# Kernel tuning notes

Hardware: AMD Instinct MI355X
Metric: run time of the kernel (lower is better)

## Reference

```python
import jax, jax.numpy as jnp
import numpy as np

B, H, W = 2, 32, 128
HW = H * W
N, C = 4096, 64
KQ, KN = 32, 16          # nsample_q, nsample
DIST = 10.0              # neighbor distance threshold
NEG = -1e10


def _knn(q, p, k):
    # q: (B,M,3), p: (B,N,3) -> idx (B,M,k), sqdist (B,M,k)
    sqd = jnp.sum((q[:, :, None, :] - p[:, None, :, :]) ** 2, axis=-1)
    neg, idx = jax.lax.top_k(-sqd, k)
    return idx, -neg


def _gather(p, idx):
    # p: (B,N,C), idx: (B,M,K) -> (B,M,K,C)
    return jax.vmap(lambda a, i: a[i])(p, idx)


def _norm_feat(x):
    # per-point channel normalization, torch.std default is unbiased (ddof=1)
    m = jnp.mean(x, axis=-1, keepdims=True)
    s = jnp.clip(jnp.std(x, axis=-1, keepdims=True, ddof=1), 1e-12)
    return (x - m) / s


def _conv(x, w, b, g, e):
    # 1x1 conv + BatchNorm (track_running_stats=False -> batch stats) + LeakyReLU(0.1)
    y = jnp.einsum('bnkc,cd->bnkd', x, w) + b
    mu = y.mean(axis=(0, 1, 2), keepdims=True)
    var = y.var(axis=(0, 1, 2), keepdims=True)
    y = (y - mu) * jax.lax.rsqrt(var + 1e-5) * g + e
    return jnp.where(y > 0, y, 0.1 * y)


def setup_inputs() -> dict:
    key = jax.random.key(0)
    ks = jax.random.split(key, 20)
    inp = {
        'xyz_proj_raw': jax.random.normal(ks[0], (B, H, W, 3), jnp.float32),
        'warped_xyz': jax.random.normal(ks[1], (B, HW, 3), jnp.float32),
        'warped_points': jax.random.normal(ks[2], (B, HW, C), jnp.float32),
        'idx_n2': jax.random.randint(ks[3], (B, HW, 2), 0, W),
        'f2_xyz': jax.random.normal(ks[4], (B, N, 3), jnp.float32),
        'f2_points': jax.random.normal(ks[5], (B, N, C), jnp.float32),
        'lidar_z': jax.random.uniform(ks[6], (B, HW, 1), jnp.float32),
    }
    shapes = {
        'm1w0': (70, 128), 'm1w1': (128, 64), 'piw': (6, 64),
        'm2w0': (128, 64), 'm2w1': (64, 64), 'pcw': (10, 64),
        'm3w0': (192, 64), 'm3w1': (64, 64),
    }
    i = 7
    for name, shp in shapes.items():
        inp[name] = jax.random.normal(ks[i], shp, jnp.float32) * 0.05
        i += 1
        pre = name[:-2] if name[-2] == 'w' else name[:-1]
        suf = name[-1] if name[-2] == 'w' else ''
        cout = shp[1]
        inp[pre + 'b' + suf] = jnp.zeros((cout,), jnp.float32)
        inp[pre + 'g' + suf] = jnp.ones((cout,), jnp.float32)
        inp[pre + 'e' + suf] = jnp.zeros((cout,), jnp.float32)
    return inp


def reference(xyz_proj_raw, warped_xyz, warped_points, idx_n2, f2_xyz, f2_points, lidar_z,
              m1w0, m1b0, m1g0, m1e0, m1w1, m1b1, m1g1, m1e1,
              piw, pib, pig, pie,
              m2w0, m2b0, m2g0, m2e0, m2w1, m2b1, m2g1, m2e1,
              pcw, pcb, pcg, pce,
              m3w0, m3b0, m3g0, m3e0, m3w1, m3b1, m3g1, m3e1):
    # ---- stage 1: cross kNN grouping into image features ----
    idx_q, _ = _knn(warped_xyz, f2_xyz, KQ)
    qi_xyz = _gather(f2_xyz, idx_q)          # (B,HW,KQ,3)
    qi_pts = _gather(f2_points, idx_q)       # (B,HW,KQ,C)

    wxyz = warped_xyz * lidar_z              # (B,HW,3)
    pi_xyz_exp = jnp.broadcast_to(wxyz[:, :, None, :], (B, HW, KQ, 3))
    pi_pts_exp = jnp.broadcast_to(warped_points[:, :, None, :], (B, HW, KQ, C))
    pi_xyz_diff_concat = jnp.concatenate([pi_xyz_exp, qi_xyz], axis=3)  # (B,HW,KQ,6)

    pi_feat_diff = _norm_feat(pi_pts_exp) * _norm_feat(qi_pts)          # correlation
    feat = jnp.concatenate([pi_xyz_diff_concat, pi_feat_diff], axis=3)  # (B,HW,KQ,70)

    feat = _conv(feat, m1w0, m1b0, m1g0, m1e0)
    feat = _conv(feat, m1w1, m1b1, m1g1, m1e1)                          # (B,HW,KQ,64)
    pi_enc = _conv(pi_xyz_diff_concat, piw, pib, pig, pie)              # (B,HW,KQ,64)

    pi_cat = jnp.concatenate([pi_enc, feat], axis=3)
    pi_cat = _conv(pi_cat, m2w0, m2b0, m2g0, m2e0)
    pi_cat = _conv(pi_cat, m2w1, m2b1, m2g1, m2e1)
    WQ = jax.nn.softmax(pi_cat, axis=2)
    pi_feat1 = jnp.sum(WQ * feat, axis=2)                               # (B,HW,64)

    # ---- stage 2: self kNN (use_trans=False -> raw projected xyz), thresholded validity ----
    xyz_pr = xyz_proj_raw.reshape(B, HW, 3)
    idx2, sqd2 = _knn(xyz_pr, xyz_pr, KN)
    valid = (sqd2 < DIST * DIST).astype(pi_feat1.dtype)[..., None]      # (B,HW,KN,1)

    pc_xyz_g = _gather(wxyz, idx2)                                      # (B,HW,KN,3)
    pc_pts_g = _gather(pi_feat1, idx2)                                  # (B,HW,KN,64)
    pc_xyz_new = jnp.broadcast_to(wxyz[:, :, None, :], (B, HW, KN, 3))
    pc_pts_new = jnp.broadcast_to(warped_points[:, :, None, :], (B, HW, KN, C))

    pc_diff = pc_xyz_g - pc_xyz_new
    pc_euc = jnp.sqrt(jnp.sum(pc_diff * pc_diff, axis=3, keepdims=True) + 1e-20)
    pc_xyz_cat = jnp.concatenate([pc_xyz_new, pc_xyz_g, pc_diff, pc_euc], axis=3)  # 10ch

    pc_enc = _conv(pc_xyz_cat, pcw, pcb, pcg, pce)
    pc_cat = jnp.concatenate([pc_enc, pc_pts_new, pc_pts_g], axis=-1)   # (B,HW,KN,192)
    pc_cat = _conv(pc_cat, m3w0, m3b0, m3g0, m3e0)
    pc_cat = _conv(pc_cat, m3w1, m3b1, m3g1, m3e1)

    pc_cat = pc_cat * valid + NEG * (1.0 - valid)
    WP = jax.nn.softmax(pc_cat, axis=2)
    out = jnp.sum(WP * pc_pts_g, axis=2)                                # (B,HW,64)
    return out.reshape(B, H, W, -1)
```

## Files before the change

### kernel.cpp

```cpp
#include <hip/hip_runtime.h>
#include <math.h>

constexpr int Bn  = 2;
constexpr int HWn = 4096;
constexpr int Nn  = 4096;
constexpr int KQn = 32;
constexpr int KNn = 16;
constexpr float INV_R1 = 1.0f/262144.0f;
constexpr float INV_R2 = 1.0f/131072.0f;

typedef _Float16 f16x8 __attribute__((ext_vector_type(8)));
typedef _Float16 f16x2 __attribute__((ext_vector_type(2)));
typedef float    f32x4 __attribute__((ext_vector_type(4)));

__device__ __forceinline__ float wred64(float v){
  #pragma unroll
  for (int m = 32; m > 0; m >>= 1) v += __shfl_xor(v, m, 64);
  return v;
}
__device__ __forceinline__ float leakyf(float v){ return v > 0.f ? v : 0.1f*v; }

__device__ __forceinline__ void bn_param(const float* st, int c, float inv_n,
                                         const float* g, const float* e,
                                         float& sc, float& sh){
  float mu  = st[c]*inv_n;
  float var = st[128+c]*inv_n - mu*mu;
  float s   = g[c]*rsqrtf(var + 1e-5f);
  sc = s; sh = e[c] - mu*s;
}

constexpr int XT_LD = 104;
__device__ __forceinline__ void build_xtile(
    int m0, const float* __restrict__ wxyz, const float* __restrict__ f2_xyz,
    const float* __restrict__ normW, const float* __restrict__ normF2,
    const int* __restrict__ idxq, _Float16* __restrict__ xt, int tid)
{
  int r = tid >> 2, q = tid & 3;
  int row = m0 + r;
  int p = row >> 5, b = p >> 12;
  int idx = idxq[row];
  unsigned int* d32 = (unsigned int*)(xt + r*XT_LD);
  union { unsigned int u; _Float16 h[2]; } pk;
  if (q == 0){
    const float* wx = wxyz + (size_t)p*3;
    const float* fx = f2_xyz + ((size_t)b*Nn + idx)*3;
    pk.h[0]=(_Float16)wx[0]; pk.h[1]=(_Float16)wx[1]; d32[0]=pk.u;
    pk.h[0]=(_Float16)wx[2]; pk.h[1]=(_Float16)fx[0]; d32[1]=pk.u;
    pk.h[0]=(_Float16)fx[1]; pk.h[1]=(_Float16)fx[2]; d32[2]=pk.u;
  }
  const float4* nw = (const float4*)(normW  + (size_t)p*64) + q*4;
  const float4* nf = (const float4*)(normF2 + ((size_t)b*Nn + idx)*64) + q*4;
  #pragma unroll
  for (int i=0;i<4;i++){
    float4 a = nw[i], f = nf[i];
    int base = 3 + q*8 + i*2;
    pk.h[0]=(_Float16)(a.x*f.x); pk.h[1]=(_Float16)(a.y*f.y); d32[base]=pk.u;
    pk.h[0]=(_Float16)(a.z*f.z); pk.h[1]=(_Float16)(a.w*f.w); d32[base+1]=pk.u;
  }
  if (q == 3){
    #pragma unroll
    for (int c=35;c<48;c++) d32[c] = 0u;
  }
}

__device__ __forceinline__ void build_x10(int row,
    const float* __restrict__ wxyz, const int* __restrict__ idx2, float* x){
  int p = row >> 4, b = p >> 12;
  int idx = idx2[row];
  const float* nw = wxyz + (size_t)p*3;
  const float* gw = wxyz + ((size_t)b*HWn + idx)*3;
  float n0=nw[0],n1=nw[1],n2=nw[2];
  float g0=gw[0],g1=gw[1],g2=gw[2];
  float d0=g0-n0, d1=g1-n1, d2=g2-n2;
  x[0]=n0;x[1]=n1;x[2]=n2; x[3]=g0;x[4]=g1;x[5]=g2;
  x[6]=d0;x[7]=d1;x[8]=d2; x[9]=sqrtf(d0*d0+d1*d1+d2*d2+1e-20f);
}

__global__ __launch_bounds__(256) void k_knn_prep(
    const float* __restrict__ qA, const float* __restrict__ pA, int* __restrict__ oA,
    const float* __restrict__ qB, const float* __restrict__ pB, int* __restrict__ oB,
    float* __restrict__ ovalid,
    const float* __restrict__ lidar_z,
    const float* __restrict__ warped_points, const float* __restrict__ f2_points,
    const float* __restrict__ m1w0, const float* __restrict__ m1w1,
    const float* __restrict__ piw, const float* __restrict__ pcw,
    const float* __restrict__ m2w0, const float* __restrict__ m2w1,
    const float* __restrict__ m3w0, const float* __restrict__ m3w1,
    float* __restrict__ wxyz, float* __restrict__ normW, float* __restrict__ normF2,
    float* __restrict__ piwT, float* __restrict__ pcwT,
    _Float16* __restrict__ w1h, _Float16* __restrict__ w2h,
    _Float16* __restrict__ w3h, _Float16* __restrict__ w4h,
    _Float16* __restrict__ w5h, _Float16* __restrict__ w6h)
{
  int bid = blockIdx.x;
  int tid = threadIdx.x;
  if (bid >= 16384){
    int blk = bid - 16384;
    if (blk < 4096){
      int lane = tid & 63;
      int p = blk*4 + (tid >> 6);
      const float* src; float* dst;
      if (p < Bn*HWn){ src = warped_points + (size_t)p*64; dst = normW + (size_t)p*64; }
      else { int q = p - Bn*HWn; src = f2_points + (size_t)q*64; dst = normF2 + (size_t)q*64; }
      float x = src[lane];
      float m = wred64(x) * (1.f/64.f);
      float d = x - m;
      float ss = wred64(d*d);
      float s = fmaxf(sqrtf(ss*(1.f/63.f)), 1e-12f);
      dst[lane] = d / s;
    } else if (blk < 4192){
      int e = (blk-4096)*256 + tid;
      wxyz[e] = qA[e] * lidar_z[e/3];
    } else if (blk < 4196){
      int e = (blk-4192)*256 + tid;
      if (e < 384){ piwT[(e & 63)*6  + (e >> 6)] = piw[e]; }
      else if (e < 1024){ int f = e-384; pcwT[(f & 63)*10 + (f >> 6)] = pcw[f]; }
    } else {
      int e = (blk-4196)*256 + tid;
      if (e < 12288){
        int j = e/96, k = e - j*96;
        w1h[e] = (k < 70) ? (_Float16)m1w0[k*128 + j] : (_Float16)0.f;
      } else if (e < 20480){
        int f = e - 12288; int d = f >> 7, c = f & 127;
        w2h[f] = (_Float16)m1w1[c*64 + d];
      } else if (e < 28672){
        int f = e - 20480; int d = f >> 7, c = f & 127;
        w3h[f] = (_Float16)m2w0[c*64 + d];
      } else if (e < 32768){
        int f = e - 28672; int d = f >> 6, c = f & 63;
        w4h[f] = (_Float16)m2w1[c*64 + d];
      } else if (e < 45056){
        int f = e - 32768; int d = f/192, c = f - 192*d;
        w5h[f] = (_Float16)m3w0[c*64 + d];
      } else {
        int f = e - 45056; int d = f >> 6, c = f & 63;
        w6h[f] = (_Float16)m3w1[c*64 + d];
      }
    }
    return;
  }
  __shared__ int hist[4096];
  __shared__ int wsum[4];
  __shared__ unsigned int redm[4], redM[4];
  __shared__ int sh_sel, sh_rem, sh_cls, cnt_lt, cnt_eq;
  bool second = bid >= 8192;
  int blk = second ? (bid - 8192) : bid;
  int K = second ? KNn : KQn;
  const float* qpts = second ? qB : qA;
  const float* pts  = second ? pB : pA;
  int* oidx = second ? oB : oA;
  int b = blk >> 12;
  int qi = blk & 4095;
  int lane = tid & 63, wv = tid >> 6;
  const float* qp = qpts + ((size_t)(b*HWn+qi))*3;
  float qx=qp[0], qy=qp[1], qz=qp[2];
  const float* pb = pts + (size_t)b*Nn*3;
  unsigned int key[16];
  {
    const float4* pb4 = (const float4*)(pb + (size_t)tid*48);
    float4 v[12];
    #pragma unroll
    for (int i=0;i<12;i++) v[i] = pb4[i];
    const float* f = (const float*)v;
    #pragma unroll
    for (int i=0;i<16;i++){
      float dx = __fsub_rn(qx, f[i*3+0]);
      float dy = __fsub_rn(qy, f[i*3+1]);
      float dz = __fsub_rn(qz, f[i*3+2]);
      float d2 = __fadd_rn(__fadd_rn(__fmul_rn(dx,dx), __fmul_rn(dy,dy)), __fmul_rn(dz,dz));
      key[i] = __float_as_uint(d2);
    }
  }
  {
    int4 z = {0,0,0,0};
    #pragma unroll
    for (int j=0;j<2;j++) ((int4*)hist)[tid + j*256] = z;
  }
  unsigned int mn = key[0], mx = key[0];
  #pragma unroll
  for (int i=1;i<16;i++){ mn = min(mn, key[i]); mx = max(mx, key[i]); }
  #pragma unroll
  for (int m=32;m>0;m>>=1){
    mn = min(mn, (unsigned int)__shfl_xor((int)mn, m, 64));
    mx = max(mx, (unsigned int)__shfl_xor((int)mx, m, 64));
  }
  if (lane == 0){ redm[wv] = mn; redM[wv] = mx; }
  if (tid == 0){ cnt_lt = 0; cnt_eq = 0; }
  __syncthreads();
  mn = min(min(redm[0],redm[1]), min(redm[2],redm[3]));
  mx = max(max(redM[0],redM[1]), max(redM[2],redM[3]));
  unsigned int R = mx - mn;
  int L = (R == 0u) ? 0 : (31 - __clz(R));
  int shift = (L > 10) ? (L - 10) : 0;
  #pragma unroll
  for (int i=0;i<16;i++){
    unsigned int d = ((key[i]-mn) >> shift) & 2047u;
    int slot = (int)(((d & 7u) << 8) | (d >> 3));
    atomicAdd(&hist[slot], 1);
  }
  __syncthreads();
  {
    int hv[8]; int tot = 0;
    #pragma unroll
    for (int i=0;i<8;i++){ hv[i] = hist[tid + i*256]; tot += hv[i]; }
    int pref = tot;
    #pragma unroll
    for (int m=1;m<64;m<<=1){ int t = __shfl_up(pref, m, 64); if (lane >= m) pref += t; }
    if (lane == 63) wsum[wv] = pref;
    __syncthreads();
    int off = 0;
    #pragma unroll
    for (int i=0;i<3;i++) if (i < wv) off += wsum[i];
    pref += off;
    if (pref >= K && (pref - tot) < K){
      int running = pref - tot;
      bool done = false;
      #pragma unroll
      for (int i=0;i<8;i++){
        if (!done && running + hv[i] >= K){
          sh_sel = tid*8 + i;
          sh_rem = K - running;
          sh_cls = hv[i];
          done = true;
        }
        if (!done) running += hv[i];
      }
    }
  }
  __syncthreads();
  unsigned int sel = (unsigned int)sh_sel;
  int rem = sh_rem, cls = sh_cls;
  int nless = K - rem;
  size_t obase = ((size_t)(b*HWn+qi))*K;
  const unsigned int U100 = __float_as_uint(100.0f);
  #pragma unroll
  for (int i=0;i<16;i++){
    unsigned int d = ((key[i]-mn) >> shift) & 2047u;
    if (d < sel){
      int s = atomicAdd(&cnt_lt, 1);
      oidx[obase+s] = tid*16 + i;
      if (second) ovalid[obase+s] = (key[i] < U100) ? 1.f : 0.f;
    } else if (d == sel){
      int s = atomicAdd(&cnt_eq, 1);
      if (s < 2048){ hist[s] = (int)key[i]; hist[2048+s] = tid*16 + i; }
    }
  }
  __syncthreads();
  if (wv == 0){
    int cc = cls < 2048 ? cls : 2048;
    for (int c = lane; c < cc; c += 64){
      unsigned int kc = (unsigned int)hist[c];
      int ic = hist[2048+c];
      int rank = 0;
      for (int j = 0; j < cc; j++){
        unsigned int kj = (unsigned int)hist[j];
        if (kj < kc || (kj == kc && hist[2048+j] < ic)) rank++;
      }
      if (rank < rem){
        oidx[obase + nless + rank] = ic;
        if (second) ovalid[obase + nless + rank] = (kc < U100) ? 1.f : 0.f;
      }
    }
  }
}

__global__ __launch_bounds__(256) void k_build_stats(
    const float* __restrict__ wxyz, const float* __restrict__ f2_xyz,
    const float* __restrict__ normW, const float* __restrict__ normF2,
    const int* __restrict__ idxq, const int* __restrict__ idx2,
    const _Float16* __restrict__ w1h,
    float* stats, float* __restrict__ gram)
{
  __shared__ float sacc[66];
  int blk = blockIdx.x, tid = threadIdx.x, lane = tid & 63;
  if (blk < 1024){
    __shared__ _Float16 xt[64*XT_LD];
    __shared__ float ssum[128], sssq[128];
    if (tid < 128){ ssum[tid]=0.f; sssq[tid]=0.f; }
    int wave = tid >> 6;
    int quad = lane >> 4, n16 = lane & 15;
    float r1[8], r2[8];
    #pragma unroll
    for (int i=0;i<8;i++){ r1[i]=0.f; r2[i]=0.f; }
    for (int t=0;t<4;t++){
      build_xtile(blk*256 + t*64, wxyz, f2_xyz, normW, normF2, idxq, xt, tid);
      __syncthreads();
      const _Float16* xr = xt + (size_t)(wave*16 + n16)*XT_LD + quad*8;
      f16x8 a0 = *(const f16x8*)(xr);
      f16x8 a1 = *(const f16x8*)(xr + 32);
      f16x8 a2 = *(const f16x8*)(xr + 64);
      #pragma unroll
      for (int nt = 0; nt < 8; nt++){
        const _Float16* wr = w1h + (size_t)(nt*16 + n16)*96 + quad*8;
        f16x8 b0 = *(const f16x8*)(wr);
        f16x8 b1 = *(const f16x8*)(wr + 32);
        f16x8 b2 = *(const f16x8*)(wr + 64);
        f32x4 acc = {0.f,0.f,0.f,0.f};
        acc = __builtin_amdgcn_mfma_f32_16x16x32_f16(a0, b0, acc, 0,0,0);
        acc = __builtin_amdgcn_mfma_f32_16x16x32_f16(a1, b1, acc, 0,0,0);
        acc = __builtin_amdgcn_mfma_f32_16x16x32_f16(a2, b2, acc, 0,0,0);
        float s1 = acc[0]+acc[1]+acc[2]+acc[3];
        float s2 = acc[0]*acc[0]+acc[1]*acc[1]+acc[2]*acc[2]+acc[3]*acc[3];
        s1 += __shfl_xor(s1, 16, 64); s1 += __shfl_xor(s1, 32, 64);
        s2 += __shfl_xor(s2, 16, 64); s2 += __shfl_xor(s2, 32, 64);
        r1[nt] += s1; r2[nt] += s2;
      }
      __syncthreads();
    }
    if (quad == 0){
      #pragma unroll
      for (int nt=0;nt<8;nt++){
        atomicAdd(&ssum[nt*16+n16], r1[nt]); atomicAdd(&sssq[nt*16+n16], r2[nt]);
      }
    }
    __syncthreads();
    if (tid < 128){ atomicAdd(&stats[tid], ssum[tid]); atomicAdd(&stats[128+tid], sssq[tid]); }
  } else if (blk < 1088){
    float a[28];
    #pragma unroll
    for (int q=0;q<28;q++) a[q]=0.f;
    int g = (blk-1024)*256 + tid;
    for (int s=0;s<16;s++){
      int row = g + s*16384;
      int p = row >> 5, b = p >> 12;
      int idx = idxq[row];
      const float* wx = wxyz + (size_t)p*3;
      const float* fx = f2_xyz + ((size_t)b*Nn + idx)*3;
      float xt7[7] = {wx[0],wx[1],wx[2],fx[0],fx[1],fx[2],1.f};
      int q=0;
      #pragma unroll
      for (int i=0;i<7;i++)
        #pragma unroll
        for (int j=i;j<7;j++) a[q++] += xt7[i]*xt7[j];
    }
    if (tid < 28) sacc[tid]=0.f;
    __syncthreads();
    #pragma unroll
    for (int q=0;q<28;q++){
      float v = wred64(a[q]);
      if (lane==0) atomicAdd(&sacc[q], v);
    }
    __syncthreads();
    if (tid < 28) atomicAdd(&gram[tid], sacc[tid]);
  } else {
    float a[66];
    #pragma unroll
    for (int q=0;q<66;q++) a[q]=0.f;
    int g = (blk-1088)*256 + tid;
    for (int s=0;s<16;s++){
      int row = g + s*8192;
      float x[10];
      build_x10(row, wxyz, idx2, x);
      float xt11[11] = {x[0],x[1],x[2],x[3],x[4],x[5],x[6],x[7],x[8],x[9],1.f};
      int q=0;
      #pragma unroll
      for (int i=0;i<11;i++)
        #pragma unroll
        for (int j=i;j<11;j++) a[q++] += xt11[i]*xt11[j];
    }
    if (tid < 66) sacc[tid]=0.f;
    __syncthreads();
    #pragma unroll
    for (int q=0;q<66;q++){
      float v = wred64(a[q]);
      if (lane==0) atomicAdd(&sacc[q], v);
    }
    __syncthreads();
    if (tid < 66) atomicAdd(&gram[32+tid], sacc[tid]);
  }
}

__global__ __launch_bounds__(256) void k_mfma_m1(
    const float* __restrict__ wxyz, const float* __restrict__ f2_xyz,
    const float* __restrict__ normW, const float* __restrict__ normF2,
    const int* __restrict__ idxq,
    const _Float16* __restrict__ w1h, const _Float16* __restrict__ w2h,
    const float* __restrict__ m1g0, const float* __restrict__ m1e0,
    float* stats, _Float16* __restrict__ y2h,
    const float* __restrict__ gram,
    const float* __restrict__ piw, const float* __restrict__ pib,
    const float* __restrict__ pcw, const float* __restrict__ pcb)
{
  if (blockIdx.x >= 1024){
    int tid = threadIdx.x;
    if (tid < 64){
      int c = tid;
      float wt[7];
      #pragma unroll
      for (int i=0;i<6;i++) wt[i] = piw[i*64+c];
      wt[6] = pib[c];
      const float* G = gram;
      float sum=0.f, ssq=0.f;
      #pragma unroll
      for (int i=0;i<7;i++){
        int offi = i*7 - (i*(i-1))/2;
        sum += wt[i]*G[offi + (6-i)];
        #pragma unroll
        for (int j=0;j<7;j++){
          int ii = i<j? i : j, jj = i<j? j : i;
          int o = ii*7 - (ii*(ii-1))/2 + (jj-ii);
          ssq += wt[i]*wt[j]*G[o];
        }
      }
      stats[2*256+c] = sum; stats[2*256+128+c] = ssq;
    } else if (tid < 128){
      int c = tid-64;
      float wt[11];
      #pragma unroll
      for (int i=0;i<10;i++) wt[i] = pcw[i*64+c];
      wt[10] = pcb[c];
      const float* G = gram + 32;
      float sum=0.f, ssq=0.f;
      #pragma unroll
      for (int i=0;i<11;i++){
        int offi = i*11 - (i*(i-1))/2;
        sum += wt[i]*G[offi + (10-i)];
        #pragma unroll
        for (int j=0;j<11;j++){
          int ii = i<j? i : j, jj = i<j? j : i;
          int o = ii*11 - (ii*(ii-1))/2 + (jj-ii);
          ssq += wt[i]*wt[j]*G[o];
        }
      }
      stats[5*256+c] = sum; stats[5*256+128+c] = ssq;
    }
    return;
  }
  __shared__ _Float16 xt[64*XT_LD];
  __shared__ _Float16 st[64*136];
  __shared__ float sc1[128], sh1[128], ssum[64], sssq[64];
  int tid = threadIdx.x;
  if (tid < 128){
    float s,h; bn_param(stats, tid, INV_R1, m1g0, m1e0, s, h);
    sc1[tid]=s; sh1[tid]=h;
  }
  if (tid < 64){ ssum[tid]=0.f; sssq[tid]=0.f; }
  int wave = tid >> 6, lane = tid & 63;
  int quad = lane >> 4, n16 = lane & 15;
  float r1[4], r2[4];
  #pragma unroll
  for (int i=0;i<4;i++){ r1[i]=0.f; r2[i]=0.f; }
  for (int t=0;t<4;t++){
    build_xtile(blockIdx.x*256 + t*64, wxyz, f2_xyz, normW, normF2, idxq, xt, tid);
    __syncthreads();
    const _Float16* xr = xt + (size_t)(wave*16 + n16)*XT_LD + quad*8;
    f16x8 a0 = *(const f16x8*)(xr);
    f16x8 a1 = *(const f16x8*)(xr + 32);
    f16x8 a2 = *(const f16x8*)(xr + 64);
    #pragma unroll
    for (int nt = 0; nt < 8; nt++){
      const _Float16* wr = w1h + (size_t)(nt*16 + n16)*96 + quad*8;
      f16x8 b0 = *(const f16x8*)(wr);
      f16x8 b1 = *(const f16x8*)(wr + 32);
      f16x8 b2 = *(const f16x8*)(wr + 64);
      f32x4 acc = {0.f,0.f,0.f,0.f};
      acc = __builtin_amdgcn_mfma_f32_16x16x32_f16(a0, b0, acc, 0,0,0);
      acc = __builtin_amdgcn_mfma_f32_16x16x32_f16(a1, b1, acc, 0,0,0);
      acc = __builtin_amdgcn_mfma_f32_16x16x32_f16(a2, b2, acc, 0,0,0);
      int ch = nt*16 + n16;
      float sc = sc1[ch], sh = sh1[ch];
      #pragma unroll
      for (int r=0;r<4;r++){
        float v = leakyf(acc[r]*sc + sh);
        st[(size_t)(wave*16 + quad*4 + r)*136 + ch] = (_Float16)v;
      }
    }
    __syncthreads();
    const _Float16* tr = st + (size_t)(wave*16 + n16)*136 + quad*8;
    f16x8 t0 = *(const f16x8*)(tr);
    f16x8 t1 = *(const f16x8*)(tr + 32);
    f16x8 t2 = *(const f16x8*)(tr + 64);
    f16x8 t3 = *(const f16x8*)(tr + 96);
    #pragma unroll
    for (int nt = 0; nt < 4; nt++){
      const _Float16* wr = w2h + (size_t)(nt*16 + n16)*128 + quad*8;
      f16x8 b0 = *(const f16x8*)(wr);
      f16x8 b1 = *(const f16x8*)(wr + 32);
      f16x8 b2 = *(const f16x8*)(wr + 64);
      f16x8 b3 = *(const f16x8*)(wr + 96);
      f32x4 acc = {0.f,0.f,0.f,0.f};
      acc = __builtin_amdgcn_mfma_f32_16x16x32_f16(t0, b0, acc, 0,0,0);
      acc = __builtin_amdgcn_mfma_f32_16x16x32_f16(t1, b1, acc, 0,0,0);
      acc = __builtin_amdgcn_mfma_f32_16x16x32_f16(t2, b2, acc, 0,0,0);
      acc = __builtin_amdgcn_mfma_f32_16x16x32_f16(t3, b3, acc, 0,0,0);
      int ch = nt*16 + n16;
      #pragma unroll
      for (int r=0;r<4;r++){
        int rowg = blockIdx.x*256 + t*64 + wave*16 + quad*4 + r;
        y2h[(size_t)rowg*64 + ch] = (_Float16)acc[r];
      }
      float s1 = acc[0]+acc[1]+acc[2]+acc[3];
      float s2 = acc[0]*acc[0]+acc[1]*acc[1]+acc[2]*acc[2]+acc[3]*acc[3];
      s1 += __shfl_xor(s1, 16, 64); s1 += __shfl_xor(s1, 32, 64);
      s2 += __shfl_xor(s2, 16, 64); s2 += __shfl_xor(s2, 32, 64);
      r1[nt] += s1; r2[nt] += s2;
    }
  }
  __syncthreads();
  if (quad == 0){
    #pragma unroll
    for (int nt=0;nt<4;nt++){
      atomicAdd(&ssum[nt*16+n16], r1[nt]); atomicAdd(&sssq[nt*16+n16], r2[nt]);
    }
  }
  __syncthreads();
  if (tid < 64){ atomicAdd(&stats[1*256+tid], ssum[tid]); atomicAdd(&stats[1*256+128+tid], sssq[tid]); }
}

__global__ __launch_bounds__(256) void k_mfma_m2a(
    const float* __restrict__ wxyz, const float* __restrict__ f2_xyz,
    const int* __restrict__ idxq,
    const float* __restrict__ piwT, const float* __restrict__ pib,
    const float* __restrict__ pig, const float* __restrict__ pie,
    const float* __restrict__ m1g1, const float* __restrict__ m1e1,
    const _Float16* __restrict__ y2h, const _Float16* __restrict__ w3h,
    float* stats, _Float16* __restrict__ y3h)
{
  __shared__ _Float16 su[64*136];
  __shared__ float spw[384];
  __shared__ float scp[64], shp[64], sc2[64], sh2[64], ssum[64], sssq[64];
  int tid = threadIdx.x;
  for (int d = tid; d < 384; d += 256) spw[d] = piwT[d];
  if (tid < 64){
    float s,h;
    bn_param(stats+2*256, tid, INV_R1, pig,  pie,  s, h); scp[tid]=s; shp[tid]=h;
    bn_param(stats+1*256, tid, INV_R1, m1g1, m1e1, s, h); sc2[tid]=s; sh2[tid]=h;
    ssum[tid]=0.f; sssq[tid]=0.f;
  }
  __syncthreads();
  int r = tid & 63, cg = tid >> 6;
  int wave = tid >> 6, lane = tid & 63, quad = lane >> 4, n16 = lane & 15;
  float r1[4], r2[4];
  #pragma unroll
  for (int i=0;i<4;i++){ r1[i]=0.f; r2[i]=0.f; }
  for (int t=0;t<4;t++){
    int rowg = blockIdx.x*256 + t*64 + r;
    {
      int p = rowg >> 5, b = p >> 12;
      int idx = idxq[rowg];
      const float* wx = wxyz + (size_t)p*3;
      const float* fx = f2_xyz + ((size_t)b*Nn + idx)*3;
      float x0=wx[0],x1=wx[1],x2=wx[2],x3=fx[0],x4=fx[1],x5=fx[2];
      #pragma unroll
      for (int jj=0;jj<16;jj++){
        int j = cg*16 + jj;
        const float* pw = spw + j*6;
        float e = pib[j] + x0*pw[0]+x1*pw[1]+x2*pw[2]+x3*pw[3]+x4*pw[4]+x5*pw[5];
        su[r*136 + j] = (_Float16)leakyf(e*scp[j] + shp[j]);
      }
      const f16x8* yr = (const f16x8*)(y2h + (size_t)rowg*64 + cg*16);
      f16x8 q0 = yr[0], q1 = yr[1];
      #pragma unroll
      for (int jj=0;jj<8;jj++){
        int c = cg*16 + jj;
        su[r*136 + 64 + c] = (_Float16)leakyf((float)q0[jj]*sc2[c] + sh2[c]);
      }
      #pragma unroll
      for (int jj=0;jj<8;jj++){
        int c = cg*16 + 8 + jj;
        su[r*136 + 64 + c] = (_Float16)leakyf((float)q1[jj]*sc2[c] + sh2[c]);
      }
    }
    __syncthreads();
    const _Float16* ur = su + (size_t)(wave*16 + n16)*136 + quad*8;
    f16x8 a0 = *(const f16x8*)(ur);
    f16x8 a1 = *(const f16x8*)(ur + 32);
    f16x8 a2 = *(const f16x8*)(ur + 64);
    f16x8 a3 = *(const f16x8*)(ur + 96);
    #pragma unroll
    for (int nt = 0; nt < 4; nt++){
      const _Float16* wr = w3h + (size_t)(nt*16 + n16)*128 + quad*8;
      f16x8 b0 = *(const f16x8*)(wr);
      f16x8 b1 = *(const f16x8*)(wr + 32);
      f16x8 b2 = *(const f16x8*)(wr + 64);
      f16x8 b3 = *(const f16x8*)(wr + 96);
      f32x4 acc = {0.f,0.f,0.f,0.f};
      acc = __builtin_amdgcn_mfma_f32_16x16x32_f16(a0, b0, acc, 0,0,0);
      acc = __builtin_amdgcn_mfma_f32_16x16x32_f16(a1, b1, acc, 0,0,0);
      acc = __builtin_amdgcn_mfma_f32_16x16x32_f16(a2, b2, acc, 0,0,0);
      acc = __builtin_amdgcn_mfma_f32_16x16x32_f16(a3, b3, acc, 0,0,0);
      int ch = nt*16 + n16;
      #pragma unroll
      for (int rr=0;rr<4;rr++){
        int rg = blockIdx.x*256 + t*64 + wave*16 + quad*4 + rr;
        y3h[(size_t)rg*64 + ch] = (_Float16)acc[rr];
      }
      float s1 = acc[0]+acc[1]+acc[2]+acc[3];
      float s2 = acc[0]*acc[0]+acc[1]*acc[1]+acc[2]*acc[2]+acc[3]*acc[3];
      s1 += __shfl_xor(s1, 16, 64); s1 += __shfl_xor(s1, 32, 64);
      s2 += __shfl_xor(s2, 16, 64); s2 += __shfl_xor(s2, 32, 64);
      r1[nt] += s1; r2[nt] += s2;
    }
    __syncthreads();
  }
  if (quad == 0){
    #pragma unroll
    for (int nt=0;nt<4;nt++){
      atomicAdd(&ssum[nt*16+n16], r1[nt]); atomicAdd(&sssq[nt*16+n16], r2[nt]);
    }
  }
  __syncthreads();
  if (tid < 64){ atomicAdd(&stats[3*256+tid], ssum[tid]); atomicAdd(&stats[3*256+128+tid], sssq[tid]); }
}

__global__ __launch_bounds__(256) void k_mfma_pw64(
    const _Float16* __restrict__ yin, const _Float16* __restrict__ wh,
    const float* __restrict__ g, const float* __restrict__ e,
    const float* statsIn, float* statsOut, float inv_n,
    _Float16* __restrict__ yout)
{
  __shared__ _Float16 stt[64*72];
  __shared__ float sc[64], sh[64], ssum[64], sssq[64];
  int tid = threadIdx.x;
  if (tid < 64){
    float s,h; bn_param(statsIn, tid, inv_n, g, e, s, h);
    sc[tid]=s; sh[tid]=h; ssum[tid]=0.f; sssq[tid]=0.f;
  }
  __syncthreads();
  int r = tid & 63, cg = tid >> 6;
  int wave = tid >> 6, lane = tid & 63, quad = lane >> 4, n16 = lane & 15;
  float r1[4], r2[4];
  #pragma unroll
  for (int i=0;i<4;i++){ r1[i]=0.f; r2[i]=0.f; }
  for (int t=0;t<4;t++){
    int rowg = blockIdx.x*256 + t*64 + r;
    const f16x8* yr = (const f16x8*)(yin + (size_t)rowg*64 + cg*16);
    f16x8 q0 = yr[0], q1 = yr[1];
    #pragma unroll
    for (int jj=0;jj<8;jj++){
      int c = cg*16 + jj;
      stt[r*72 + c] = (_Float16)leakyf((float)q0[jj]*sc[c] + sh[c]);
    }
    #pragma unroll
    for (int jj=0;jj<8;jj++){
      int c = cg*16 + 8 + jj;
      stt[r*72 + c] = (_Float16)leakyf((float)q1[jj]*sc[c] + sh[c]);
    }
    __syncthreads();
    const _Float16* tr = stt + (size_t)(wave*16 + n16)*72 + quad*8;
    f16x8 a0 = *(const f16x8*)(tr);
    f16x8 a1 = *(const f16x8*)(tr + 32);
    #pragma unroll
    for (int nt = 0; nt < 4; nt++){
      const _Float16* wr = wh + (size_t)(nt*16 + n16)*64 + quad*8;
      f16x8 b0 = *(const f16x8*)(wr);
      f16x8 b1 = *(const f16x8*)(wr + 32);
      f32x4 acc = {0.f,0.f,0.f,0.f};
      acc = __builtin_amdgcn_mfma_f32_16x16x32_f16(a0, b0, acc, 0,0,0);
      acc = __builtin_amdgcn_mfma_f32_16x16x32_f16(a1, b1, acc, 0,0,0);
      int ch = nt*16 + n16;
      #pragma unroll
      for (int rr=0;rr<4;rr++){
        int rg = blockIdx.x*256 + t*64 + wave*16 + quad*4 + rr;
        yout[(size_t)rg*64 + ch] = (_Float16)acc[rr];
      }
      float s1 = acc[0]+acc[1]+acc[2]+acc[3];
      float s2 = acc[0]*acc[0]+acc[1]*acc[1]+acc[2]*acc[2]+acc[3]*acc[3];
      s1 += __shfl_xor(s1, 16, 64); s1 += __shfl_xor(s1, 32, 64);
      s2 += __shfl_xor(s2, 16, 64); s2 += __shfl_xor(s2, 32, 64);
      r1[nt] += s1; r2[nt] += s2;
    }
    __syncthreads();
  }
  if (quad == 0){
    #pragma unroll
    for (int nt=0;nt<4;nt++){
      atomicAdd(&ssum[nt*16+n16], r1[nt]); atomicAdd(&sssq[nt*16+n16], r2[nt]);
    }
  }
  __syncthreads();
  if (tid < 64){ atomicAdd(&statsOut[tid], ssum[tid]); atomicAdd(&statsOut[128+tid], sssq[tid]); }
}

__global__ __launch_bounds__(256) void k_mfma_m3a(
    const float* __restrict__ wxyz, const float* __restrict__ warped_points,
    const _Float16* __restrict__ pif1h, const int* __restrict__ idx2,
    const float* __restrict__ pcwT, const float* __restrict__ pcb,
    const float* __restrict__ pcg, const float* __restrict__ pce,
    const _Float16* __restrict__ w5h,
    float* stats, _Float16* __restrict__ y5h)
{
  __shared__ _Float16 sv[64*200];
  __shared__ float spw[640];
  __shared__ float scp[64], shp[64], ssum[64], sssq[64];
  int tid = threadIdx.x;
  for (int d = tid; d < 640; d += 256) spw[d] = pcwT[d];
  if (tid < 64){
    float s,h; bn_param(stats+5*256, tid, INV_R2, pcg, pce, s, h);
    scp[tid]=s; shp[tid]=h; ssum[tid]=0.f; sssq[tid]=0.f;
  }
  __syncthreads();
  int r = tid & 63, cg = tid >> 6;
  int wave = tid >> 6, lane = tid & 63, quad = lane >> 4, n16 = lane & 15;
  float r1[4], r2[4];
  #pragma unroll
  for (int i=0;i<4;i++){ r1[i]=0.f; r2[i]=0.f; }
  for (int t=0;t<4;t++){
    int rowg = blockIdx.x*256 + t*64 + r;
    {
      int p = rowg >> 4, b = p >> 12;
      int idx = idx2[rowg];
      float x[10];
      build_x10(rowg, wxyz, idx2, x);
      #pragma unroll
      for (int jj=0;jj<16;jj++){
        int j = cg*16 + jj;
        const float* pw = spw + j*10;
        float e = pcb[j];
        #pragma unroll
        for (int i=0;i<10;i++) e += x[i]*pw[i];
        sv[r*200 + j] = (_Float16)leakyf(e*scp[j] + shp[j]);
      }
      const float4* wp = (const float4*)(warped_points + (size_t)p*64 + cg*16);
      #pragma unroll
      for (int v4=0; v4<4; v4++){
        float4 q = wp[v4];
        int c = 64 + cg*16 + v4*4;
        sv[r*200 + c + 0] = (_Float16)q.x;
        sv[r*200 + c + 1] = (_Float16)q.y;
        sv[r*200 + c + 2] = (_Float16)q.z;
        sv[r*200 + c + 3] = (_Float16)q.w;
      }
      const f16x8* pg = (const f16x8*)(pif1h + ((size_t)(b*HWn) + idx)*64 + cg*16);
      f16x8 g0 = pg[0], g1 = pg[1];
      #pragma unroll
      for (int jj=0;jj<8;jj++) sv[r*200 + 128 + cg*16 + jj] = g0[jj];
      #pragma unroll
      for (int jj=0;jj<8;jj++) sv[r*200 + 136 + cg*16 + jj] = g1[jj];
    }
    __syncthreads();
    const _Float16* vr = sv + (size_t)(wave*16 + n16)*200 + quad*8;
    f16x8 a0 = *(const f16x8*)(vr);
    f16x8 a1 = *(const f16x8*)(vr + 32);
    f16x8 a2 = *(const f16x8*)(vr + 64);
    f16x8 a3 = *(const f16x8*)(vr + 96);
    f16x8 a4 = *(const f16x8*)(vr + 128);
    f16x8 a5 = *(const f16x8*)(vr + 160);
    #pragma unroll
    for (int nt = 0; nt < 4; nt++){
      const _Float16* wr = w5h + (size_t)(nt*16 + n16)*192 + quad*8;
      f32x4 acc = {0.f,0.f,0.f,0.f};
      acc = __builtin_amdgcn_mfma_f32_16x16x32_f16(a0, *(const f16x8*)(wr),       acc, 0,0,0);
      acc = __builtin_amdgcn_mfma_f32_16x16x32_f16(a1, *(const f16x8*)(wr + 32),  acc, 0,0,0);
      acc = __builtin_amdgcn_mfma_f32_16x16x32_f16(a2, *(const f16x8*)(wr + 64),  acc, 0,0,0);
      acc = __builtin_amdgcn_mfma_f32_16x16x32_f16(a3, *(const f16x8*)(wr + 96),  acc, 0,0,0);
      acc = __builtin_amdgcn_mfma_f32_16x16x32_f16(a4, *(const f16x8*)(wr + 128), acc, 0,0,0);
      acc = __builtin_amdgcn_mfma_f32_16x16x32_f16(a5, *(const f16x8*)(wr + 160), acc, 0,0,0);
      int ch = nt*16 + n16;
      #pragma unroll
      for (int rr=0;rr<4;rr++){
        int rg = blockIdx.x*256 + t*64 + wave*16 + quad*4 + rr;
        y5h[(size_t)rg*64 + ch] = (_Float16)acc[rr];
      }
      float s1 = acc[0]+acc[1]+acc[2]+acc[3];
      float s2 = acc[0]*acc[0]+acc[1]*acc[1]+acc[2]*acc[2]+acc[3]*acc[3];
      s1 += __shfl_xor(s1, 16, 64); s1 += __shfl_xor(s1, 32, 64);
      s2 += __shfl_xor(s2, 16, 64); s2 += __shfl_xor(s2, 32, 64);
      r1[nt] += s1; r2[nt] += s2;
    }
    __syncthreads();
  }
  if (quad == 0){
    #pragma unroll
    for (int nt=0;nt<4;nt++){
      atomicAdd(&ssum[nt*16+n16], r1[nt]); atomicAdd(&sssq[nt*16+n16], r2[nt]);
    }
  }
  __syncthreads();
  if (tid < 64){ atomicAdd(&stats[6*256+tid], ssum[tid]); atomicAdd(&stats[6*256+128+tid], sssq[tid]); }
}

__global__ __launch_bounds__(256) void k_softmax1(
    const _Float16* __restrict__ y2h, const _Float16* __restrict__ y4h,
    const float* stats,
    const float* __restrict__ m1g1, const float* __restrict__ m1e1,
    const float* __restrict__ m2g1, const float* __restrict__ m2e1,
    _Float16* __restrict__ pif1h)
{
  int tid = threadIdx.x;
  int p  = blockIdx.x*8 + (tid >> 5);
  int dp = tid & 31;
  int d0 = 2*dp, d1 = 2*dp + 1;
  float sc2a,sh2a,sc4a,sh4a, sc2b,sh2b,sc4b,sh4b;
  bn_param(stats+1*256, d0, INV_R1, m1g1, m1e1, sc2a, sh2a);
  bn_param(stats+4*256, d0, INV_R1, m2g1, m2e1, sc4a, sh4a);
  bn_param(stats+1*256, d1, INV_R1, m1g1, m1e1, sc2b, sh2b);
  bn_param(stats+4*256, d1, INV_R1, m2g1, m2e1, sc4b, sh4b);
  size_t rb = (size_t)p*KQn;
  const _Float16* y4base = y4h + rb*64 + d0;
  const _Float16* y2base = y2h + rb*64 + d0;
  float va[32], vb[32];
  float mxa = -1e30f, mxb = -1e30f;
  #pragma unroll
  for (int k=0;k<32;k++){
    f16x2 h = *(const f16x2*)(y4base + (size_t)k*64);
    float ta = leakyf((float)h[0]*sc4a + sh4a);
    float tb = leakyf((float)h[1]*sc4b + sh4b);
    va[k] = ta; mxa = fmaxf(mxa, ta);
    vb[k] = tb; mxb = fmaxf(mxb, tb);
  }
  float sea = 0.f, seb = 0.f;
  #pragma unroll
  for (int k=0;k<32;k++){
    float ea = __expf(va[k]-mxa); va[k]=ea; sea += ea;
    float eb = __expf(vb[k]-mxb); vb[k]=eb; seb += eb;
  }
  float inva = 1.f/sea, invb = 1.f/seb;
  float acca = 0.f, accb = 0.f;
  #pragma unroll
  for (int k=0;k<32;k++){
    f16x2 h = *(const f16x2*)(y2base + (size_t)k*64);
    acca += va[k]*leakyf((float)h[0]*sc2a + sh2a);
    accb += vb[k]*leakyf((float)h[1]*sc2b + sh2b);
  }
  f16x2 o; o[0] = (_Float16)(acca*inva); o[1] = (_Float16)(accb*invb);
  *(f16x2*)(pif1h + (size_t)p*64 + d0) = o;
}

__global__ __launch_bounds__(256) void k_softmax2(
    const _Float16* __restrict__ y6h, const _Float16* __restrict__ pif1h,
    const int* __restrict__ idx2, const float* __restrict__ validf,
    const float* stats,
    const float* __restrict__ m3g1, const float* __restrict__ m3e1,
    float* __restrict__ out)
{
  int tid = threadIdx.x;
  int p  = blockIdx.x*8 + (tid >> 5);
  int b  = p >> 12;
  int dp = tid & 31;
  int d0 = 2*dp, d1 = 2*dp + 1;
  float sca,sha,scb,shb;
  bn_param(stats+7*256, d0, INV_R2, m3g1, m3e1, sca, sha);
  bn_param(stats+7*256, d1, INV_R2, m3g1, m3e1, scb, shb);
  size_t rb = (size_t)p*KNn;
  const _Float16* y6base = y6h + rb*64 + d0;
  float va[16], vb[16];
  float mxa = -1e30f, mxb = -1e30f;
  #pragma unroll
  for (int k=0;k<16;k++){
    f16x2 h = *(const f16x2*)(y6base + (size_t)k*64);
    bool ok = validf[rb+k] > 0.5f;
    float ta = ok ? leakyf((float)h[0]*sca + sha) : -1e10f;
    float tb = ok ? leakyf((float)h[1]*scb + shb) : -1e10f;
    va[k] = ta; mxa = fmaxf(mxa, ta);
    vb[k] = tb; mxb = fmaxf(mxb, tb);
  }
  float sea = 0.f, seb = 0.f;
  #pragma unroll
  for (int k=0;k<16;k++){
    float ea = __expf(va[k]-mxa); va[k]=ea; sea += ea;
    float eb = __expf(vb[k]-mxb); vb[k]=eb; seb += eb;
  }
  float inva = 1.f/sea, invb = 1.f/seb;
  float acca = 0.f, accb = 0.f;
  #pragma unroll
  for (int k=0;k<16;k++){
    int idx = idx2[rb+k];
    f16x2 h = *(const f16x2*)(pif1h + ((size_t)(b*HWn) + idx)*64 + d0);
    acca += va[k]*(float)h[0];
    accb += vb[k]*(float)h[1];
  }
  float2 o; o.x = acca*inva; o.y = accb*invb;
  *(float2*)(out + (size_t)p*64 + d0) = o;
}

extern "C" void kernel_launch(void* const* d_in, const int* in_sizes, int n_in,
                              void* d_out, int out_size, void* d_ws, size_t ws_size,
                              hipStream_t stream)
{
  (void)in_sizes; (void)n_in; (void)out_size; (void)ws_size;
  const float* xyz_proj      = (const float*)d_in[0];
  const float* warped_xyz    = (const float*)d_in[1];
  const float* warped_points = (const float*)d_in[2];
  const float* f2_xyz        = (const float*)d_in[4];
  const float* f2_points     = (const float*)d_in[5];
  const float* lidar_z       = (const float*)d_in[6];
  const float* m1w0=(const float*)d_in[7],  *m1g0=(const float*)d_in[9],  *m1e0=(const float*)d_in[10];
  const float* m1w1=(const float*)d_in[11], *m1g1=(const float*)d_in[13], *m1e1=(const float*)d_in[14];
  const float* piw =(const float*)d_in[15], *pib =(const float*)d_in[16], *pig =(const float*)d_in[17], *pie =(const float*)d_in[18];
  const float* m2w0=(const float*)d_in[19], *m2g0=(const float*)d_in[21], *m2e0=(const float*)d_in[22];
  const float* m2w1=(const float*)d_in[23], *m2g1=(const float*)d_in[25], *m2e1=(const float*)d_in[26];
  const float* pcw =(const float*)d_in[27], *pcb =(const float*)d_in[28], *pcg =(const float*)d_in[29], *pce =(const float*)d_in[30];
  const float* m3w0=(const float*)d_in[31], *m3g0=(const float*)d_in[33], *m3e0=(const float*)d_in[34];
  const float* m3w1=(const float*)d_in[35], *m3g1=(const float*)d_in[37], *m3e1=(const float*)d_in[38];
  float* out = (float*)d_out;

  float* ws     = (float*)d_ws;
  float* wxyz   = ws;
  float* normW  = wxyz   + 24576;
  float* normF2 = normW  + 524288;
  float* piwT   = normF2 + 524288;
  float* pcwT   = piwT   + 384;
  float* stats  = pcwT   + 640;
  float* gram   = stats  + 2048;
  int*   idxq   = (int*)(gram + 128);
  int*   idx2   = idxq   + 262144;
  float* validf = (float*)(idx2 + 131072);
  _Float16* pif1h = (_Float16*)(validf + 131072);
  float* X1f    = validf + 131072 + 524288;
  float* y2f    = X1f + 12582912;
  _Float16* y2h = (_Float16*)y2f;
  float* y3f    = y2f + 8388608;
  _Float16* y3h = (_Float16*)y3f;
  float* whb    = y3f + 8388608;
  _Float16* w1h = (_Float16*)whb;
  _Float16* w2h = w1h + 12288;
  _Float16* w3h = w2h + 8192;
  _Float16* w4h = w3h + 8192;
  _Float16* w5h = w4h + 4096;
  _Float16* w6h = w5h + 12288;
  _Float16* y4h = (_Float16*)X1f;
  _Float16* y5h = (_Float16*)(X1f + 8388608);
  _Float16* y6h = y3h;

  hipMemsetAsync(stats, 0, (2048+128)*sizeof(float), stream);
  k_knn_prep<<<20772,256,0,stream>>>(warped_xyz, f2_xyz, idxq,
                                     xyz_proj, xyz_proj, idx2, validf,
                                     lidar_z, warped_points, f2_points,
                                     m1w0, m1w1, piw, pcw, m2w0, m2w1, m3w0, m3w1,
                                     wxyz, normW, normF2, piwT, pcwT,
                                     w1h, w2h, w3h, w4h, w5h, w6h);
  k_build_stats<<<1120,256,0,stream>>>(wxyz, f2_xyz, normW, normF2, idxq, idx2,
                                       w1h, stats, gram);
  k_mfma_m1<<<1025,256,0,stream>>>(wxyz, f2_xyz, normW, normF2, idxq,
                                   w1h, w2h, m1g0, m1e0, stats, y2h,
                                   gram, piw, pib, pcw, pcb);
  k_mfma_m2a<<<1024,256,0,stream>>>(wxyz, f2_xyz, idxq, piwT, pib, pig, pie,
                                    m1g1, m1e1, y2h, w3h, stats, y3h);
  k_mfma_pw64<<<1024,256,0,stream>>>(y3h, w4h, m2g0, m2e0,
                                     stats+3*256, stats+4*256, INV_R1, y4h);
  k_softmax1<<<1024,256,0,stream>>>(y2h, y4h, stats, m1g1, m1e1, m2g1, m2e1, pif1h);
  k_mfma_m3a<<<512,256,0,stream>>>(wxyz, warped_points, pif1h, idx2,
                                   pcwT, pcb, pcg, pce, w5h, stats, y5h);
  k_mfma_pw64<<<512,256,0,stream>>>(y5h, w6h, m3g0, m3e0,
                                    stats+6*256, stats+7*256, INV_R2, y6h);
  k_softmax2<<<1024,256,0,stream>>>(y6h, pif1h, idx2, validf, stats, m3g1, m3e1, out);
}
```

Baseline: 492.5 us.

## Fuse post-KNN kernel chain into one cooperative persistent kernel with grid syncs

Replaces the eight separate launches that follow the KNN prep (stats, m1, m2a, pw64, softmax1, m3a, pw64, softmax2) with a single cooperative kernel of 512 blocks. Each phase loops over work items and the phases are separated by grid.sync and thread fences, with a shared-memory arena reused across phases. The aim is to remove per-launch overhead and inter-kernel gaps. In exchange, occupancy is capped at 512 persistent blocks, a grid-wide barrier is paid at every phase, and some cross-phase stores use atomics. A fallback path with separate kernels runs when a cooperative launch is not possible.

Measured after the change: 572.3 us. 16.2% more time.

```diff
diff --git a/kernel.cpp b/kernel.cpp
--- a/kernel.cpp
+++ b/kernel.cpp
@@ -1,5 +1,8 @@
 #include <hip/hip_runtime.h>
+#include <hip/hip_cooperative_groups.h>
 #include <math.h>
+
+namespace cg = cooperative_groups;
 
 constexpr int Bn  = 2;
 constexpr int HWn = 4096;
@@ -264,18 +267,30 @@
   }
 }
 
-__global__ __launch_bounds__(256) void k_build_stats(
-    const float* __restrict__ wxyz, const float* __restrict__ f2_xyz,
-    const float* __restrict__ normW, const float* __restrict__ normF2,
-    const int* __restrict__ idxq, const int* __restrict__ idx2,
-    const _Float16* __restrict__ w1h,
-    float* stats, float* __restrict__ gram)
-{
-  __shared__ float sacc[66];
-  int blk = blockIdx.x, tid = threadIdx.x, lane = tid & 63;
+struct ChainArgs {
+  const float *wxyz, *f2_xyz, *normW, *normF2;
+  const int *idxq, *idx2;
+  const _Float16 *w1h, *w2h, *w3h, *w4h, *w5h, *w6h;
+  float *stats, *gram;
+  const float *piwT, *pcwT;
+  const float *piw, *pib, *pig, *pie;
+  const float *pcw, *pcb, *pcg, *pce;
+  const float *m1g0, *m1e0, *m1g1, *m1e1;
+  const float *m2g0, *m2e0, *m2g1, *m2e1;
+  const float *m3g0, *m3e0, *m3g1, *m3e1;
+  const float *warped_points, *validf;
+  _Float16 *y2h, *y3h, *y4h, *y5h, *y6h, *pif1h;
+  float *out;
+};
+
+constexpr int ARENA = 29440;
+
+__device__ void phase0(const ChainArgs& A, char* sm, int blk, int tid){
+  int lane = tid & 63;
   if (blk < 1024){
-    __shared__ _Float16 xt[64*XT_LD];
-    __shared__ float ssum[128], sssq[128];
+    _Float16* xt  = (_Float16*)sm;
+    float* ssum = (float*)(sm + 13312);
+    float* sssq = (float*)(sm + 13824);
     if (tid < 128){ ssum[tid]=0.f; sssq[tid]=0.f; }
     int wave = tid >> 6;
     int quad = lane >> 4, n16 = lane & 15;
@@ -283,7 +298,7 @@
     #pragma unroll
     for (int i=0;i<8;i++){ r1[i]=0.f; r2[i]=0.f; }
     for (int t=0;t<4;t++){
-      build_xtile(blk*256 + t*64, wxyz, f2_xyz, normW, normF2, idxq, xt, tid);
+      build_xtile(blk*256 + t*64, A.wxyz, A.f2_xyz, A.normW, A.normF2, A.idxq, xt, tid);
       __syncthreads();
       const _Float16* xr = xt + (size_t)(wave*16 + n16)*XT_LD + quad*8;
       f16x8 a0 = *(const f16x8*)(xr);
@@ -291,7 +306,7 @@
       f16x8 a2 = *(const f16x8*)(xr + 64);
       #pragma unroll
       for (int nt = 0; nt < 8; nt++){
-        const _Float16* wr = w1h + (size_t)(nt*16 + n16)*96 + quad*8;
+        const _Float16* wr = A.w1h + (size_t)(nt*16 + n16)*96 + quad*8;
         f16x8 b0 = *(const f16x8*)(wr);
         f16x8 b1 = *(const f16x8*)(wr + 32);
         f16x8 b2 = *(const f16x8*)(wr + 64);
@@ -314,8 +329,9 @@
       }
     }
     __syncthreads();
-    if (tid < 128){ atomicAdd(&stats[tid], ssum[tid]); atomicAdd(&stats[128+tid], sssq[tid]); }
+    if (tid < 128){ atomicAdd(&A.stats[tid], ssum[tid]); atomicAdd(&A.stats[128+tid], sssq[tid]); }
   } else if (blk < 1088){
+    float* sacc = (float*)(sm + 14336);
     float a[28];
     #pragma unroll
     for (int q=0;q<28;q++) a[q]=0.f;
@@ -323,9 +339,9 @@
     for (int s=0;s<16;s++){
       int row = g + s*16384;
       int p = row >> 5, b = p >> 12;
-      int idx = idxq[row];
-      const float* wx = wxyz + (size_t)p*3;
-      const float* fx = f2_xyz + ((size_t)b*Nn + idx)*3;
+      int idx = A.idxq[row];
+      const float* wx = A.wxyz + (size_t)p*3;
+      const float* fx = A.f2_xyz + ((size_t)b*Nn + idx)*3;
       float xt7[7] = {wx[0],wx[1],wx[2],fx[0],fx[1],fx[2],1.f};
       int q=0;
       #pragma unroll
@@ -341,8 +357,10 @@
       if (lane==0) atomicAdd(&sacc[q], v);
     }
     __syncthreads();
-    if (tid < 28) atomicAdd(&gram[tid], sacc[tid]);
+    if (tid < 28) atomicAdd(&A.gram[tid], sacc[tid]);
+    __syncthreads();
   } else {
+    float* sacc = (float*)(sm + 14336);
     float a[66];
     #pragma unroll
     for (int q=0;q<66;q++) a[q]=0.f;
@@ -350,7 +368,7 @@
     for (int s=0;s<16;s++){
       int row = g + s*8192;
       float x[10];
-      build_x10(row, wxyz, idx2, x);
+      build_x10(row, A.wxyz, A.idx2, x);
       float xt11[11] = {x[0],x[1],x[2],x[3],x[4],x[5],x[6],x[7],x[8],x[9],1.f};
       int q=0;
       #pragma unroll
@@ -366,72 +384,66 @@
       if (lane==0) atomicAdd(&sacc[q], v);
     }
     __syncthreads();
-    if (tid < 66) atomicAdd(&gram[32+tid], sacc[tid]);
-  }
-}
-
-__global__ __launch_bounds__(256) void k_mfma_m1(
-    const float* __restrict__ wxyz, const float* __restrict__ f2_xyz,
-    const float* __restrict__ normW, const float* __restrict__ normF2,
-    const int* __restrict__ idxq,
-    const _Float16* __restrict__ w1h, const _Float16* __restrict__ w2h,
-    const float* __restrict__ m1g0, const float* __restrict__ m1e0,
-    float* stats, _Float16* __restrict__ y2h,
-    const float* __restrict__ gram,
-    const float* __restrict__ piw, const float* __restrict__ pib,
-    const float* __restrict__ pcw, const float* __restrict__ pcb)
-{
-  if (blockIdx.x >= 1024){
-    int tid = threadIdx.x;
-    if (tid < 64){
-      int c = tid;
-      float wt[7];
-      #pragma unroll
-      for (int i=0;i<6;i++) wt[i] = piw[i*64+c];
-      wt[6] = pib[c];
-      const float* G = gram;
-      float sum=0.f, ssq=0.f;
-      #pragma unroll
-      for (int i=0;i<7;i++){
-        int offi = i*7 - (i*(i-1))/2;
-        sum += wt[i]*G[offi + (6-i)];
-        #pragma unroll
-        for (int j=0;j<7;j++){
-          int ii = i<j? i : j, jj = i<j? j : i;
-          int o = ii*7 - (ii*(ii-1))/2 + (jj-ii);
-          ssq += wt[i]*wt[j]*G[o];
-        }
-      }
-      stats[2*256+c] = sum; stats[2*256+128+c] = ssq;
-    } else if (tid < 128){
-      int c = tid-64;
-      float wt[11];
-      #pragma unroll
-      for (int i=0;i<10;i++) wt[i] = pcw[i*64+c];
-      wt[10] = pcb[c];
-      const float* G = gram + 32;
-      float sum=0.f, ssq=0.f;
-      #pragma unroll
-      for (int i=0;i<11;i++){
-        int offi = i*11 - (i*(i-1))/2;
-        sum += wt[i]*G[offi + (10-i)];
-        #pragma unroll
-        for (int j=0;j<11;j++){
-          int ii = i<j? i : j, jj = i<j? j : i;
-          int o = ii*11 - (ii*(ii-1))/2 + (jj-ii);
-          ssq += wt[i]*wt[j]*G[o];
-        }
-      }
-      stats[5*256+c] = sum; stats[5*256+128+c] = ssq;
-    }
-    return;
-  }
-  __shared__ _Float16 xt[64*XT_LD];
-  __shared__ _Float16 st[64*136];
-  __shared__ float sc1[128], sh1[128], ssum[64], sssq[64];
-  int tid = threadIdx.x;
+    if (tid < 66) atomicAdd(&A.gram[32+tid], sacc[tid]);
+    __syncthreads();
+  }
+}
+
+__device__ void gram_fin(const ChainArgs& A, int tid){
+  if (tid < 64){
+    int c = tid;
+    float wt[7];
+    #pragma unroll
+    for (int i=0;i<6;i++) wt[i] = A.piw[i*64+c];
+    wt[6] = A.pib[c];
+    const float* G = A.gram;
+    float sum=0.f, ssq=0.f;
+    #pragma unroll
+    for (int i=0;i<7;i++){
+      int offi = i*7 - (i*(i-1))/2;
+      sum += wt[i]*G[offi + (6-i)];
+      #pragma unroll
+      for (int j=0;j<7;j++){
+        int ii = i<j? i : j, jj = i<j? j : i;
+        int o = ii*7 - (ii*(ii-1))/2 + (jj-ii);
+        ssq += wt[i]*wt[j]*G[o];
+      }
+    }
+    __hip_atomic_store(&A.stats[2*256+c], sum, __ATOMIC_RELAXED, __HIP_MEMORY_SCOPE_AGENT);
+    __hip_atomic_store(&A.stats[2*256+128+c], ssq, __ATOMIC_RELAXED, __HIP_MEMORY_SCOPE_AGENT);
+  } else if (tid < 128){
+    int c = tid-64;
+    float wt[11];
+    #pragma unroll
+    for (int i=0;i<10;i++) wt[i] = A.pcw[i*64+c];
+    wt[10] = A.pcb[c];
+    const float* G = A.gram + 32;
+    float sum=0.f, ssq=0.f;
+    #pragma unroll
+    for (int i=0;i<11;i++){
+      int offi = i*11 - (i*(i-1))/2;
+      sum += wt[i]*G[offi + (10-i)];
+      #pragma unroll
+      for (int j=0;j<11;j++){
+        int ii = i<j? i : j, jj = i<j? j : i;
+        int o = ii*11 - (ii*(ii-1))/2 + (jj-ii);
+        ssq += wt[i]*wt[j]*G[o];
+      }
+    }
+    __hip_atomic_store(&A.stats[5*256+c], sum, __ATOMIC_RELAXED, __HIP_MEMORY_SCOPE_AGENT);
+    __hip_atomic_store(&A.stats[5*256+128+c], ssq, __ATOMIC_RELAXED, __HIP_MEMORY_SCOPE_AGENT);
+  }
+}
+
+__device__ void phase1_m1(const ChainArgs& A, char* sm, int w, int tid){
+  _Float16* xt  = (_Float16*)sm;
+  _Float16* st  = (_Float16*)sm;
+  float* sc1  = (float*)(sm + 17408);
+  float* sh1  = (float*)(sm + 17920);
+  float* ssum = (float*)(sm + 18432);
+  float* sssq = (float*)(sm + 18688);
   if (tid < 128){
-    float s,h; bn_param(stats, tid, INV_R1, m1g0, m1e0, s, h);
+    float s,h; bn_param(A.stats, tid, INV_R1, A.m1g0, A.m1e0, s, h);
     sc1[tid]=s; sh1[tid]=h;
   }
   if (tid < 64){ ssum[tid]=0.f; sssq[tid]=0.f; }
@@ -441,15 +453,16 @@
   #pragma unroll
   for (int i=0;i<4;i++){ r1[i]=0.f; r2[i]=0.f; }
   for (int t=0;t<4;t++){
-    build_xtile(blockIdx.x*256 + t*64, wxyz, f2_xyz, normW, normF2, idxq, xt, tid);
+    build_xtile(w*256 + t*64, A.wxyz, A.f2_xyz, A.normW, A.normF2, A.idxq, xt, tid);
     __syncthreads();
     const _Float16* xr = xt + (size_t)(wave*16 + n16)*XT_LD + quad*8;
     f16x8 a0 = *(const f16x8*)(xr);
     f16x8 a1 = *(const f16x8*)(xr + 32);
     f16x8 a2 = *(const f16x8*)(xr + 64);
+    __syncthreads();
     #pragma unroll
     for (int nt = 0; nt < 8; nt++){
-      const _Float16* wr = w1h + (size_t)(nt*16 + n16)*96 + quad*8;
+      const _Float16* wr = A.w1h + (size_t)(nt*16 + n16)*96 + quad*8;
       f16x8 b0 = *(const f16x8*)(wr);
       f16x8 b1 = *(const f16x8*)(wr + 32);
       f16x8 b2 = *(const f16x8*)(wr + 64);
@@ -473,7 +486,7 @@
     f16x8 t3 = *(const f16x8*)(tr + 96);
     #pragma unroll
     for (int nt = 0; nt < 4; nt++){
-      const _Float16* wr = w2h + (size_t)(nt*16 + n16)*128 + quad*8;
+      const _Float16* wr = A.w2h + (size_t)(nt*16 + n16)*128 + quad*8;
       f16x8 b0 = *(const f16x8*)(wr);
       f16x8 b1 = *(const f16x8*)(wr + 32);
       f16x8 b2 = *(const f16x8*)(wr + 64);
@@ -486,8 +499,8 @@
       int ch = nt*16 + n16;
       #pragma unroll
       for (int r=0;r<4;r++){
-        int rowg = blockIdx.x*256 + t*64 + wave*16 + quad*4 + r;
-        y2h[(size_t)rowg*64 + ch] = (_Float16)acc[r];
+        int rowg = w*256 + t*64 + wave*16 + quad*4 + r;
+        A.y2h[(size_t)rowg*64 + ch] = (_Float16)acc[r];
       }
       float s1 = acc[0]+acc[1]+acc[2]+acc[3];
       float s2 = acc[0]*acc[0]+acc[1]*acc[1]+acc[2]*acc[2]+acc[3]*acc[3];
@@ -495,8 +508,8 @@
       s2 += __shfl_xor(s2, 16, 64); s2 += __shfl_xor(s2, 32, 64);
       r1[nt] += s1; r2[nt] += s2;
     }
-  }
-  __syncthreads();
+    __syncthreads();
+  }
   if (quad == 0){
     #pragma unroll
     for (int nt=0;nt<4;nt++){
@@ -504,60 +517,56 @@
     }
   }
   __syncthreads();
-  if (tid < 64){ atomicAdd(&stats[1*256+tid], ssum[tid]); atomicAdd(&stats[1*256+128+tid], sssq[tid]); }
-}
-
-__global__ __launch_bounds__(256) void k_mfma_m2a(
-    const float* __restrict__ wxyz, const float* __restrict__ f2_xyz,
-    const int* __restrict__ idxq,
-    const float* __restrict__ piwT, const float* __restrict__ pib,
-    const float* __restrict__ pig, const float* __restrict__ pie,
-    const float* __restrict__ m1g1, const float* __restrict__ m1e1,
-    const _Float16* __restrict__ y2h, const _Float16* __restrict__ w3h,
-    float* stats, _Float16* __restrict__ y3h)
-{
-  __shared__ _Float16 su[64*136];
-  __shared__ float spw[384];
-  __shared__ float scp[64], shp[64], sc2[64], sh2[64], ssum[64], sssq[64];
-  int tid = threadIdx.x;
-  for (int d = tid; d < 384; d += 256) spw[d] = piwT[d];
+  if (tid < 64){ atomicAdd(&A.stats[1*256+tid], ssum[tid]); atomicAdd(&A.stats[1*256+128+tid], sssq[tid]); }
+}
+
+__device__ void phase2_m2a(const ChainArgs& A, char* sm, int w, int tid){
+  _Float16* su = (_Float16*)sm;
+  float* spw = (float*)(sm + 17408);
+  float* scp = (float*)(sm + 18944);
+  float* shp = (float*)(sm + 19200);
+  float* sc2 = (float*)(sm + 19456);
+  float* sh2 = (float*)(sm + 19712);
+  float* ssum = (float*)(sm + 19968);
+  float* sssq = (float*)(sm + 20224);
+  for (int d = tid; d < 384; d += 256) spw[d] = A.piwT[d];
   if (tid < 64){
     float s,h;
-    bn_param(stats+2*256, tid, INV_R1, pig,  pie,  s, h); scp[tid]=s; shp[tid]=h;
-    bn_param(stats+1*256, tid, INV_R1, m1g1, m1e1, s, h); sc2[tid]=s; sh2[tid]=h;
+    bn_param(A.stats+2*256, tid, INV_R1, A.pig,  A.pie,  s, h); scp[tid]=s; shp[tid]=h;
+    bn_param(A.stats+1*256, tid, INV_R1, A.m1g1, A.m1e1, s, h); sc2[tid]=s; sh2[tid]=h;
     ssum[tid]=0.f; sssq[tid]=0.f;
   }
   __syncthreads();
-  int r = tid & 63, cg = tid >> 6;
+  int r = tid & 63, cgp = tid >> 6;
   int wave = tid >> 6, lane = tid & 63, quad = lane >> 4, n16 = lane & 15;
   float r1[4], r2[4];
   #pragma unroll
   for (int i=0;i<4;i++){ r1[i]=0.f; r2[i]=0.f; }
   for (int t=0;t<4;t++){
-    int rowg = blockIdx.x*256 + t*64 + r;
+    int rowg = w*256 + t*64 + r;
     {
       int p = rowg >> 5, b = p >> 12;
-      int idx = idxq[rowg];
-      const float* wx = wxyz + (size_t)p*3;
-      const float* fx = f2_xyz + ((size_t)b*Nn + idx)*3;
+      int idx = A.idxq[rowg];
+      const float* wx = A.wxyz + (size_t)p*3;
+      const float* fx = A.f2_xyz + ((size_t)b*Nn + idx)*3;
       float x0=wx[0],x1=wx[1],x2=wx[2],x3=fx[0],x4=fx[1],x5=fx[2];
       #pragma unroll
       for (int jj=0;jj<16;jj++){
-        int j = cg*16 + jj;
+        int j = cgp*16 + jj;
         const float* pw = spw + j*6;
-        float e = pib[j] + x0*pw[0]+x1*pw[1]+x2*pw[2]+x3*pw[3]+x4*pw[4]+x5*pw[5];
+        float e = A.pib[j] + x0*pw[0]+x1*pw[1]+x2*pw[2]+x3*pw[3]+x4*pw[4]+x5*pw[5];
         su[r*136 + j] = (_Float16)leakyf(e*scp[j] + shp[j]);
       }
-      const f16x8* yr = (const f16x8*)(y2h + (size_t)rowg*64 + cg*16);
+      const f16x8* yr = (const f16x8*)(A.y2h + (size_t)rowg*64 + cgp*16);
       f16x8 q0 = yr[0], q1 = yr[1];
       #pragma unroll
       for (int jj=0;jj<8;jj++){
-        int c = cg*16 + jj;
+        int c = cgp*16 + jj;
         su[r*136 + 64 + c] = (_Float16)leakyf((float)q0[jj]*sc2[c] + sh2[c]);
       }
       #pragma unroll
       for (int jj=0;jj<8;jj++){
-        int c = cg*16 + 8 + jj;
+        int c = cgp*16 + 8 + jj;
         su[r*136 + 64 + c] = (_Float16)leakyf((float)q1[jj]*sc2[c] + sh2[c]);
       }
     }
@@ -569,7 +578,7 @@
     f16x8 a3 = *(const f16x8*)(ur + 96);
     #pragma unroll
     for (int nt = 0; nt < 4; nt++){
-      const _Float16* wr = w3h + (size_t)(nt*16 + n16)*128 + quad*8;
+      const _Float16* wr = A.w3h + (size_t)(nt*16 + n16)*128 + quad*8;
       f16x8 b0 = *(const f16x8*)(wr);
       f16x8 b1 = *(const f16x8*)(wr + 32);
       f16x8 b2 = *(const f16x8*)(wr + 64);
@@ -582,8 +591,8 @@
       int ch = nt*16 + n16;
       #pragma unroll
       for (int rr=0;rr<4;rr++){
-        int rg = blockIdx.x*256 + t*64 + wave*16 + quad*4 + rr;
-        y3h[(size_t)rg*64 + ch] = (_Float16)acc[rr];
+        int rg = w*256 + t*64 + wave*16 + quad*4 + rr;
+        A.y3h[(size_t)rg*64 + ch] = (_Float16)acc[rr];
       }
       float s1 = acc[0]+acc[1]+acc[2]+acc[3];
       float s2 = acc[0]*acc[0]+acc[1]*acc[1]+acc[2]*acc[2]+acc[3]*acc[3];
@@ -600,40 +609,42 @@
     }
   }
   __syncthreads();
-  if (tid < 64){ atomicAdd(&stats[3*256+tid], ssum[tid]); atomicAdd(&stats[3*256+128+tid], sssq[tid]); }
-}
-
-__global__ __launch_bounds__(256) void k_mfma_pw64(
+  if (tid < 64){ atomicAdd(&A.stats[3*256+tid], ssum[tid]); atomicAdd(&A.stats[3*256+128+tid], sssq[tid]); }
+}
+
+__device__ void phase_pw64(char* sm, int w, int tid,
     const _Float16* __restrict__ yin, const _Float16* __restrict__ wh,
     const float* __restrict__ g, const float* __restrict__ e,
     const float* statsIn, float* statsOut, float inv_n,
     _Float16* __restrict__ yout)
 {
-  __shared__ _Float16 stt[64*72];
-  __shared__ float sc[64], sh[64], ssum[64], sssq[64];
-  int tid = threadIdx.x;
+  _Float16* stt = (_Float16*)sm;
+  float* sc  = (float*)(sm + 9216);
+  float* sh  = (float*)(sm + 9472);
+  float* ssum = (float*)(sm + 9728);
+  float* sssq = (float*)(sm + 9984);
   if (tid < 64){
     float s,h; bn_param(statsIn, tid, inv_n, g, e, s, h);
     sc[tid]=s; sh[tid]=h; ssum[tid]=0.f; sssq[tid]=0.f;
   }
   __syncthreads();
-  int r = tid & 63, cg = tid >> 6;
+  int r = tid & 63, cgp = tid >> 6;
   int wave = tid >> 6, lane = tid & 63, quad = lane >> 4, n16 = lane & 15;
   float r1[4], r2[4];
   #pragma unroll
   for (int i=0;i<4;i++){ r1[i]=0.f; r2[i]=0.f; }
   for (int t=0;t<4;t++){
-    int rowg = blockIdx.x*256 + t*64 + r;
-    const f16x8* yr = (const f16x8*)(yin + (size_t)rowg*64 + cg*16);
+    int rowg = w*256 + t*64 + r;
+    const f16x8* yr = (const f16x8*)(yin + (size_t)rowg*64 + cgp*16);
     f16x8 q0 = yr[0], q1 = yr[1];
     #pragma unroll
     for (int jj=0;jj<8;jj++){
-      int c = cg*16 + jj;
+      int c = cgp*16 + jj;
       stt[r*72 + c] = (_Float16)leakyf((float)q0[jj]*sc[c] + sh[c]);
     }
     #pragma unroll
     for (int jj=0;jj<8;jj++){
-      int c = cg*16 + 8 + jj;
+      int c = cgp*16 + 8 + jj;
       stt[r*72 + c] = (_Float16)leakyf((float)q1[jj]*sc[c] + sh[c]);
     }
     __syncthreads();
@@ -651,7 +662,7 @@
       int ch = nt*16 + n16;
       #pragma unroll
       for (int rr=0;rr<4;rr++){
-        int rg = blockIdx.x*256 + t*64 + wave*16 + quad*4 + rr;
+        int rg = w*256 + t*64 + wave*16 + quad*4 + rr;
         yout[(size_t)rg*64 + ch] = (_Float16)acc[rr];
       }
       float s1 = acc[0]+acc[1]+acc[2]+acc[3];
@@ -672,61 +683,56 @@
   if (tid < 64){ atomicAdd(&statsOut[tid], ssum[tid]); atomicAdd(&statsOut[128+tid], sssq[tid]); }
 }
 
-__global__ __launch_bounds__(256) void k_mfma_m3a(
-    const float* __restrict__ wxyz, const float* __restrict__ warped_points,
-    const _Float16* __restrict__ pif1h, const int* __restrict__ idx2,
-    const float* __restrict__ pcwT, const float* __restrict__ pcb,
-    const float* __restrict__ pcg, const float* __restrict__ pce,
-    const _Float16* __restrict__ w5h,
-    float* stats, _Float16* __restrict__ y5h)
-{
-  __shared__ _Float16 sv[64*200];
-  __shared__ float spw[640];
-  __shared__ float scp[64], shp[64], ssum[64], sssq[64];
-  int tid = threadIdx.x;
-  for (int d = tid; d < 640; d += 256) spw[d] = pcwT[d];
+__device__ void phase5_m3a(const ChainArgs& A, char* sm, int w, int tid){
+  _Float16* sv = (_Float16*)sm;
+  float* spw = (float*)(sm + 25600);
+  float* scp = (float*)(sm + 28160);
+  float* shp = (float*)(sm + 28416);
+  float* ssum = (float*)(sm + 28672);
+  float* sssq = (float*)(sm + 28928);
+  for (int d = tid; d < 640; d += 256) spw[d] = A.pcwT[d];
   if (tid < 64){
-    float s,h; bn_param(stats+5*256, tid, INV_R2, pcg, pce, s, h);
+    float s,h; bn_param(A.stats+5*256, tid, INV_R2, A.pcg, A.pce, s, h);
     scp[tid]=s; shp[tid]=h; ssum[tid]=0.f; sssq[tid]=0.f;
   }
   __syncthreads();
-  int r = tid & 63, cg = tid >> 6;
+  int r = tid & 63, cgp = tid >> 6;
   int wave = tid >> 6, lane = tid & 63, quad = lane >> 4, n16 = lane & 15;
   float r1[4], r2[4];
   #pragma unroll
   for (int i=0;i<4;i++){ r1[i]=0.f; r2[i]=0.f; }
   for (int t=0;t<4;t++){
-    int rowg = blockIdx.x*256 + t*64 + r;
+    int rowg = w*256 + t*64 + r;
     {
       int p = rowg >> 4, b = p >> 12;
-      int idx = idx2[rowg];
+      int idx = A.idx2[rowg];
       float x[10];
-      build_x10(rowg, wxyz, idx2, x);
+      build_x10(rowg, A.wxyz, A.idx2, x);
       #pragma unroll
       for (int jj=0;jj<16;jj++){
-        int j = cg*16 + jj;
+        int j = cgp*16 + jj;
         const float* pw = spw + j*10;
-        float e = pcb[j];
+        float e = A.pcb[j];
         #pragma unroll
         for (int i=0;i<10;i++) e += x[i]*pw[i];
         sv[r*200 + j] = (_Float16)leakyf(e*scp[j] + shp[j]);
       }
-      const float4* wp = (const float4*)(warped_points + (size_t)p*64 + cg*16);
+      const float4* wp = (const float4*)(A.warped_points + (size_t)p*64 + cgp*16);
       #pragma unroll
       for (int v4=0; v4<4; v4++){
         float4 q = wp[v4];
-        int c = 64 + cg*16 + v4*4;
+        int c = 64 + cgp*16 + v4*4;
         sv[r*200 + c + 0] = (_Float16)q.x;
         sv[r*200 + c + 1] = (_Float16)q.y;
         sv[r*200 + c + 2] = (_Float16)q.z;
         sv[r*200 + c + 3] = (_Float16)q.w;
       }
-      const f16x8* pg = (const f16x8*)(pif1h + ((size_t)(b*HWn) + idx)*64 + cg*16);
+      const f16x8* pg = (const f16x8*)(A.pif1h + ((size_t)(b*HWn) + idx)*64 + cgp*16);
       f16x8 g0 = pg[0], g1 = pg[1];
       #pragma unroll
-      for (int jj=0;jj<8;jj++) sv[r*200 + 128 + cg*16 + jj] = g0[jj];
-      #pragma unroll
-      for (int jj=0;jj<8;jj++) sv[r*200 + 136 + cg*16 + jj] = g1[jj];
+      for (int jj=0;jj<8;jj++) sv[r*200 + 128 + cgp*16 + jj] = g0[jj];
+      #pragma unroll
+      for (int jj=0;jj<8;jj++) sv[r*200 + 136 + cgp*16 + jj] = g1[jj];
     }
     __syncthreads();
     const _Float16* vr = sv + (size_t)(wave*16 + n16)*200 + quad*8;
@@ -738,7 +744,7 @@
     f16x8 a5 = *(const f16x8*)(vr + 160);
     #pragma unroll
     for (int nt = 0; nt < 4; nt++){
-      const _Float16* wr = w5h + (size_t)(nt*16 + n16)*192 + quad*8;
+      const _Float16* wr = A.w5h + (size_t)(nt*16 + n16)*192 + quad*8;
       f32x4 acc = {0.f,0.f,0.f,0.f};
       acc = __builtin_amdgcn_mfma_f32_16x16x32_f16(a0, *(const f16x8*)(wr),       acc, 0,0,0);
       acc = __builtin_amdgcn_mfma_f32_16x16x32_f16(a1, *(const f16x8*)(wr + 32),  acc, 0,0,0);
@@ -749,8 +755,8 @@
       int ch = nt*16 + n16;
       #pragma unroll
       for (int rr=0;rr<4;rr++){
-        int rg = blockIdx.x*256 + t*64 + wave*16 + quad*4 + rr;
-        y5h[(size_t)rg*64 + ch] = (_Float16)acc[rr];
+        int rg = w*256 + t*64 + wave*16 + quad*4 + rr;
+        A.y5h[(size_t)rg*64 + ch] = (_Float16)acc[rr];
       }
       float s1 = acc[0]+acc[1]+acc[2]+acc[3];
       float s2 = acc[0]*acc[0]+acc[1]*acc[1]+acc[2]*acc[2]+acc[3]*acc[3];
@@ -767,28 +773,21 @@
     }
   }
   __syncthreads();
-  if (tid < 64){ atomicAdd(&stats[6*256+tid], ssum[tid]); atomicAdd(&stats[6*256+128+tid], sssq[tid]); }
-}
-
-__global__ __launch_bounds__(256) void k_softmax1(
-    const _Float16* __restrict__ y2h, const _Float16* __restrict__ y4h,
-    const float* stats,
-    const float* __restrict__ m1g1, const float* __restrict__ m1e1,
-    const float* __restrict__ m2g1, const float* __restrict__ m2e1,
-    _Float16* __restrict__ pif1h)
-{
-  int tid = threadIdx.x;
-  int p  = blockIdx.x*8 + (tid >> 5);
+  if (tid < 64){ atomicAdd(&A.stats[6*256+tid], ssum[tid]); atomicAdd(&A.stats[6*256+128+tid], sssq[tid]); }
+}
+
+__device__ void phase4_softmax1(const ChainArgs& A, int w, int tid){
+  int p  = w*8 + (tid >> 5);
   int dp = tid & 31;
   int d0 = 2*dp, d1 = 2*dp + 1;
   float sc2a,sh2a,sc4a,sh4a, sc2b,sh2b,sc4b,sh4b;
-  bn_param(stats+1*256, d0, INV_R1, m1g1, m1e1, sc2a, sh2a);
-  bn_param(stats+4*256, d0, INV_R1, m2g1, m2e1, sc4a, sh4a);
-  bn_param(stats+1*256, d1, INV_R1, m1g1, m1e1, sc2b, sh2b);
-  bn_param(stats+4*256, d1, INV_R1, m2g1, m2e1, sc4b, sh4b);
+  bn_param(A.stats+1*256, d0, INV_R1, A.m1g1, A.m1e1, sc2a, sh2a);
+  bn_param(A.stats+4*256, d0, INV_R1, A.m2g1, A.m2e1, sc4a, sh4a);
+  bn_param(A.stats+1*256, d1, INV_R1, A.m1g1, A.m1e1, sc2b, sh2b);
+  bn_param(A.stats+4*256, d1, INV_R1, A.m2g1, A.m2e1, sc4b, sh4b);
   size_t rb = (size_t)p*KQn;
-  const _Float16* y4base = y4h + rb*64 + d0;
-  const _Float16* y2base = y2h + rb*64 + d0;
+  const _Float16* y4base = A.y4h + rb*64 + d0;
+  const _Float16* y2base = A.y2h + rb*64 + d0;
   float va[32], vb[32];
   float mxa = -1e30f, mxb = -1e30f;
   #pragma unroll
@@ -813,55 +812,112 @@
     acca += va[k]*leakyf((float)h[0]*sc2a + sh2a);
     accb += vb[k]*leakyf((float)h[1]*sc2b + sh2b);
   }
-  f16x2 o; o[0] = (_Float16)(acca*inva); o[1] = (_Float16)(accb*invb);
-  *(f16x2*)(pif1h + (size_t)p*64 + d0) = o;
-}
-
-__global__ __launch_bounds__(256) void k_softmax2(
-    const _Float16* __restrict__ y6h, const _Float16* __restrict__ pif1h,
-    const int* __restrict__ idx2, const float* __restrict__ validf,
-    const float* stats,
-    const float* __restrict__ m3g1, const float* __restrict__ m3e1,
-    float* __restrict__ out)
-{
-  int tid = threadIdx.x;
-  int p  = blockIdx.x*8 + (tid >> 5);
-  int b  = p >> 12;
-  int dp = tid & 31;
-  int d0 = 2*dp, d1 = 2*dp + 1;
-  float sca,sha,scb,shb;
-  bn_param(stats+7*256, d0, INV_R2, m3g1, m3e1, sca, sha);
-  bn_param(stats+7*256, d1, INV_R2, m3g1, m3e1, scb, shb);
-  size_t rb = (size_t)p*KNn;
-  const _Float16* y6base = y6h + rb*64 + d0;
-  float va[16], vb[16];
-  float mxa = -1e30f, mxb = -1e30f;
-  #pragma unroll
-  for (int k=0;k<16;k++){
-    f16x2 h = *(const f16x2*)(y6base + (size_t)k*64);
-    bool ok = validf[rb+k] > 0.5f;
-    float ta = ok ? leakyf((float)h[0]*sca + sha) : -1e10f;
-    float tb = ok ? leakyf((float)h[1]*scb + shb) : -1e10f;
-    va[k] = ta; mxa = fmaxf(mxa, ta);
-    vb[k] = tb; mxb = fmaxf(mxb, tb);
-  }
-  float sea = 0.f, seb = 0.f;
-  #pragma unroll
-  for (int k=0;k<16;k++){
-    float ea = __expf(va[k]-mxa); va[k]=ea; sea += ea;
-    float eb = __expf(vb[k]-mxb); vb[k]=eb; seb += eb;
-  }
-  float inva = 1.f/sea, invb = 1.f/seb;
-  float acca = 0.f, accb = 0.f;
-  #pragma unroll
-  for (int k=0;k<16;k++){
-    int idx = idx2[rb+k];
-    f16x2 h = *(const f16x2*)(pif1h + ((size_t)(b*HWn) + idx)*64 + d0);
-    acca += va[k]*(float)h[0];
-    accb += vb[k]*(float)h[1];
-  }
-  float2 o; o.x = acca*inva; o.y = accb*invb;
-  *(float2*)(out + (size_t)p*64 + d0) = o;
+  union { unsigned int u; _Float16 h[2]; } pk;
+  pk.h[0] = (_Float16)(acca*inva); pk.h[1] = (_Float16)(accb*invb);
+  __hip_atomic_store((unsigned int*)(A.pif1h + (size_t)p*64 + d0), pk.u,
+                     __ATOMIC_RELAXED, __HIP_MEMORY_SCOPE_AGENT);
+}
+
+__device__ void phase7_softmax2(const ChainArgs& A, int w, int tid){
+  #pragma unroll
+  for (int pp=0; pp<2; pp++){
+    int p  = w*16 + pp*8 + (tid >> 5);
+    int b  = p >> 12;
+    int dp = tid & 31;
+    int d0 = 2*dp, d1 = 2*dp + 1;
+    float sca,sha,scb,shb;
+    bn_param(A.stats+7*256, d0, INV_R2, A.m3g1, A.m3e1, sca, sha);
+    bn_param(A.stats+7*256, d1, INV_R2, A.m3g1, A.m3e1, scb, shb);
+    size_t rb = (size_t)p*KNn;
+    const _Float16* y6base = A.y6h + rb*64 + d0;
+    float va[16], vb[16];
+    float mxa = -1e30f, mxb = -1e30f;
+    #pragma unroll
+    for (int k=0;k<16;k++){
+      f16x2 h = *(const f16x2*)(y6base + (size_t)k*64);
+      bool ok = A.validf[rb+k] > 0.5f;
+      float ta = ok ? leakyf((float)h[0]*sca + sha) : -1e10f;
+      float tb = ok ? leakyf((float)h[1]*scb + shb) : -1e10f;
+      va[k] = ta; mxa = fmaxf(mxa, ta);
+      vb[k] = tb; mxb = fmaxf(mxb, tb);
+    }
+    float sea = 0.f, seb = 0.f;
+    #pragma unroll
+    for (int k=0;k<16;k++){
+      float ea = __expf(va[k]-mxa); va[k]=ea; sea += ea;
+      float eb = __expf(vb[k]-mxb); vb[k]=eb; seb += eb;
+    }
+    float inva = 1.f/sea, invb = 1.f/seb;
+    float acca = 0.f, accb = 0.f;
+    #pragma unroll
+    for (int k=0;k<16;k++){
+      int idx = A.idx2[rb+k];
+      f16x2 h = *(const f16x2*)(A.pif1h + ((size_t)(b*HWn) + idx)*64 + d0);
+      acca += va[k]*(float)h[0];
+      accb += vb[k]*(float)h[1];
+    }
+    float2 o; o.x = acca*inva; o.y = accb*invb;
+    *(float2*)(A.out + (size_t)p*64 + d0) = o;
+  }
+}
+
+__global__ __launch_bounds__(256, 2) void k_chain(ChainArgs A){
+  __shared__ __align__(16) char sm[ARENA];
+  cg::grid_group grid = cg::this_grid();
+  int bid = blockIdx.x, tid = threadIdx.x;
+  for (int w = bid; w < 1120; w += 512) phase0(A, sm, w, tid);
+  __threadfence(); grid.sync();
+  if (bid == 0) gram_fin(A, tid);
+  for (int w = bid; w < 1024; w += 512) phase1_m1(A, sm, w, tid);
+  __threadfence(); grid.sync();
+  for (int w = bid; w < 1024; w += 512) phase2_m2a(A, sm, w, tid);
+  __threadfence(); grid.sync();
+  for (int w = bid; w < 1024; w += 512)
+    phase_pw64(sm, w, tid, A.y3h, A.w4h, A.m2g0, A.m2e0,
+               A.stats+3*256, A.stats+4*256, INV_R1, A.y4h);
+  __threadfence(); grid.sync();
+  for (int w = bid; w < 1024; w += 512) phase4_softmax1(A, w, tid);
+  __threadfence(); grid.sync();
+  phase5_m3a(A, sm, bid, tid);
+  __threadfence(); grid.sync();
+  phase_pw64(sm, bid, tid, A.y5h, A.w6h, A.m3g0, A.m3e0,
+             A.stats+6*256, A.stats+7*256, INV_R2, A.y6h);
+  __threadfence(); grid.sync();
+  phase7_softmax2(A, bid, tid);
+}
+
+__global__ __launch_bounds__(256) void g_phase0(ChainArgs A){
+  __shared__ __align__(16) char sm[14608];
+  phase0(A, sm, blockIdx.x, threadIdx.x);
+}
+__global__ __launch_bounds__(256) void g_m1(ChainArgs A){
+  __shared__ __align__(16) char sm[18944];
+  if (blockIdx.x >= 1024){ gram_fin(A, threadIdx.x); return; }
+  phase1_m1(A, sm, blockIdx.x, threadIdx.x);
+}
+__global__ __launch_bounds__(256) void g_m2a(ChainArgs A){
+  __shared__ __align__(16) char sm[20480];
+  phase2_m2a(A, sm, blockIdx.x, threadIdx.x);
+}
+__global__ __launch_bounds__(256) void g_pw64a(ChainArgs A){
+  __shared__ __align__(16) char sm[10240];
+  phase_pw64(sm, blockIdx.x, threadIdx.x, A.y3h, A.w4h, A.m2g0, A.m2e0,
+             A.stats+3*256, A.stats+4*256, INV_R1, A.y4h);
+}
+__global__ __launch_bounds__(256) void g_sm1(ChainArgs A){
+  phase4_softmax1(A, blockIdx.x, threadIdx.x);
+}
+__global__ __launch_bounds__(256) void g_m3a(ChainArgs A){
+  __shared__ __align__(16) char sm[29184];
+  phase5_m3a(A, sm, blockIdx.x, threadIdx.x);
+}
+__global__ __launch_bounds__(256) void g_pw64b(ChainArgs A){
+  __shared__ __align__(16) char sm[10240];
+  phase_pw64(sm, blockIdx.x, threadIdx.x, A.y5h, A.w6h, A.m3g0, A.m3e0,
+             A.stats+6*256, A.stats+7*256, INV_R2, A.y6h);
+}
+__global__ __launch_bounds__(256) void g_sm2(ChainArgs A){
+  phase7_softmax2(A, blockIdx.x, threadIdx.x);
 }
 
 extern "C" void kernel_launch(void* const* d_in, const int* in_sizes, int n_in,
@@ -920,19 +976,45 @@
                                      m1w0, m1w1, piw, pcw, m2w0, m2w1, m3w0, m3w1,
                                      wxyz, normW, normF2, piwT, pcwT,
                                      w1h, w2h, w3h, w4h, w5h, w6h);
-  k_build_stats<<<1120,256,0,stream>>>(wxyz, f2_xyz, normW, normF2, idxq, idx2,
-                                       w1h, stats, gram);
-  k_mfma_m1<<<1025,256,0,stream>>>(wxyz, f2_xyz, normW, normF2, idxq,
-                                   w1h, w2h, m1g0, m1e0, stats, y2h,
-                                   gram, piw, pib, pcw, pcb);
-  k_mfma_m2a<<<1024,256,0,stream>>>(wxyz, f2_xyz, idxq, piwT, pib, pig, pie,
-                                    m1g1, m1e1, y2h, w3h, stats, y3h);
-  k_mfma_pw64<<<1024,256,0,stream>>>(y3h, w4h, m2g0, m2e0,
-                                     stats+3*256, stats+4*256, INV_R1, y4h);
-  k_softmax1<<<1024,256,0,stream>>>(y2h, y4h, stats, m1g1, m1e1, m2g1, m2e1, pif1h);
-  k_mfma_m3a<<<512,256,0,stream>>>(wxyz, warped_points, pif1h, idx2,
-                                   pcwT, pcb, pcg, pce, w5h, stats, y5h);
-  k_mfma_pw64<<<512,256,0,stream>>>(y5h, w6h, m3g0, m3e0,
-                                    stats+6*256, stats+7*256, INV_R2, y6h);
-  k_softmax2<<<1024,256,0,stream>>>(y6h, pif1h, idx2, validf, stats, m3g1, m3e1, out);
-}
+  ChainArgs CA;
+  CA.wxyz = wxyz; CA.f2_xyz = f2_xyz; CA.normW = normW; CA.normF2 = normF2;
+  CA.idxq = idxq; CA.idx2 = idx2;
+  CA.w1h = w1h; CA.w2h = w2h; CA.w3h = w3h; CA.w4h = w4h; CA.w5h = w5h; CA.w6h = w6h;
+  CA.stats = stats; CA.gram = gram;
+  CA.piwT = piwT; CA.pcwT = pcwT;
+  CA.piw = piw; CA.pib = pib; CA.pig = pig; CA.pie = pie;
+  CA.pcw = pcw; CA.pcb = pcb; CA.pcg = pcg; CA.pce = pce;
+  CA.m1g0 = m1g0; CA.m1e0 = m1e0; CA.m1g1 = m1g1; CA.m1e1 = m1e1;
+  CA.m2g0 = m2g0; CA.m2e0 = m2e0; CA.m2g1 = m2g1; CA.m2e1 = m2e1;
+  CA.m3g0 = m3g0; CA.m3e0 = m3e0; CA.m3g1 = m3g1; CA.m3e1 = m3e1;
+  CA.warped_points = warped_points; CA.validf = validf;
+  CA.y2h = y2h; CA.y3h = y3h; CA.y4h = y4h; CA.y5h = y5h; CA.y6h = y6h;
+  CA.pif1h = pif1h; CA.out = out;
+
+  bool coop = false;
+  {
+    int nb = 0;
+    if (hipOccupancyMaxActiveBlocksPerMultiprocessor(&nb, k_chain, 256, 0) == hipSuccess){
+      int dev = 0; hipGetDevice(&dev);
+      int cus = 0;
+      hipDeviceGetAttribute(&cus, hipDeviceAttributeMultiprocessorCount, dev);
+      if ((long)nb * (long)cus >= 512) coop = true;
+    }
+  }
+  if (coop){
+    void* kargs[] = { (void*)&CA };
+    hipError_t e = hipLaunchCooperativeKernel((const void*)k_chain, dim3(512), dim3(256),
+                                              kargs, 0u, stream);
+    if (e != hipSuccess) coop = false;
+  }
+  if (!coop){
+    g_phase0<<<1120,256,0,stream>>>(CA);
+    g_m1<<<1025,256,0,stream>>>(CA);
+    g_m2a<<<1024,256,0,stream>>>(CA);
+    g_pw64a<<<1024,256,0,stream>>>(CA);
+    g_sm1<<<1024,256,0,stream>>>(CA);
+    g_m3a<<<512,256,0,stream>>>(CA);
+    g_pw64b<<<512,256,0,stream>>>(CA);
+    g_sm2<<<512,256,0,stream>>>(CA);
+  }
+}
```
